# Performance work log

Measured on AMD Instinct MI355X. Metric: run time of the kernel, lower is better.

## Reference

```python
import jax, jax.numpy as jnp
import numpy as np

STRIDES = (8.0, 16.0, 32.0)
ANCHORS = np.array([[[10, 13], [16, 30], [33, 23]],
                    [[30, 61], [62, 45], [59, 119]],
                    [[116, 90], [156, 198], [373, 326]]], dtype=np.float32)
NC = 80
NO = NC + 5
NA = 3
CONF_THRES = 0.15
IOU_THRES = 0.45
MAX_DET = 100
TOPK = 1000          # NMS candidate pre-selection (greedy NMS over top-1000 scores)
MASK_SIZE = 28
MAX_WH = 4096.0      # class offset for batched (class-aware) NMS


def conv(x, w):
    # NCHW conv, stride 1, 'SAME' padding == torch padding=k//2
    return jax.lax.conv_general_dilated(x, w, (1, 1), 'SAME',
                                        dimension_numbers=('NCHW', 'OIHW', 'NCHW'))


def convbn(x, w, g, b, act=False):
    # Conv + (folded) BatchNorm affine + optional SiLU
    y = conv(x, w) * g[None, :, None, None] + b[None, :, None, None]
    return y * jax.nn.sigmoid(y) if act else y


def resize_ac(x, oh, ow):
    # bilinear resize, align_corners=True, NCHW
    H, W = x.shape[-2], x.shape[-1]
    ys = jnp.linspace(0.0, H - 1.0, oh)
    xs = jnp.linspace(0.0, W - 1.0, ow)
    y0 = jnp.floor(ys).astype(jnp.int32); y1 = jnp.minimum(y0 + 1, H - 1)
    x0 = jnp.floor(xs).astype(jnp.int32); x1 = jnp.minimum(x0 + 1, W - 1)
    fy = ys - y0; fx = xs - x0
    rows = x[..., y0, :] * (1.0 - fy)[:, None] + x[..., y1, :] * fy[:, None]
    return rows[..., x0] * (1.0 - fx) + rows[..., x1] * fx


def decode(fraw, anchors_px, stride):
    # fraw: [bs, na*no, ny, nx] -> [bs, na*ny*nx, no] in pixel coords
    bs, _, ny, nx = fraw.shape
    d = fraw.reshape(bs, NA, NO, ny, nx).transpose(0, 1, 3, 4, 2)  # [bs,na,ny,nx,no]
    y = jax.nn.sigmoid(d)
    yv, xv = jnp.meshgrid(jnp.arange(ny, dtype=fraw.dtype),
                          jnp.arange(nx, dtype=fraw.dtype), indexing='ij')
    grid = jnp.stack((xv, yv), -1) - 0.5                 # [ny,nx,2]
    xy = (y[..., :2] * 2.0 + grid) * stride
    wh = (y[..., 2:4] * 2.0) ** 2 * anchors_px[None, :, None, None, :]
    return jnp.concatenate((xy, wh, y[..., 4:]), -1).reshape(bs, -1, NO)


def box_iou(a, b):
    area = lambda t: (t[:, 2] - t[:, 0]) * (t[:, 3] - t[:, 1])
    lt = jnp.maximum(a[:, None, :2], b[None, :, :2])
    rb = jnp.minimum(a[:, None, 2:], b[None, :, 2:])
    wh = jnp.clip(rb - lt, 0.0)
    inter = wh[..., 0] * wh[..., 1]
    return inter / (area(a)[:, None] + area(b)[None, :] - inter + 1e-7)


def nms_image(pred):
    # pred: [N, 85]. conf = obj * cls (multi_label=False -> best class)
    xy = pred[:, :2]; wh = pred[:, 2:4]
    boxes = jnp.concatenate((xy - wh / 2.0, xy + wh / 2.0), -1)
    obj = pred[:, 4]; cls = pred[:, 5:]
    score = obj * jnp.max(cls, -1)
    cls_idx = jnp.argmax(cls, -1)
    s = jnp.where(score > CONF_THRES, score, -1.0)
    sK, idx = jax.lax.top_k(s, TOPK)
    bK = boxes[idx]; cK = cls_idx[idx]
    vK = sK > CONF_THRES
    offb = bK + (cK.astype(bK.dtype) * MAX_WH)[:, None]  # class-aware offset
    iou = box_iou(offb, offb)

    def body(i, st):
        keep, supp = st
        ki = vK[i] & jnp.logical_not(supp[i])
        supp = jnp.where(ki, jnp.logical_or(supp, iou[i] > IOU_THRES), supp)
        return keep.at[i].set(ki), supp

    keep, _ = jax.lax.fori_loop(0, TOPK, body,
                                (jnp.zeros(TOPK, dtype=bool), jnp.zeros(TOPK, dtype=bool)))
    sF = jnp.where(keep, sK, -1.0)
    top_s, top_i = jax.lax.top_k(sF, MAX_DET)
    valid = top_s > 0.0
    out_boxes = bK[top_i] * valid[:, None]
    out_scores = jnp.where(valid, top_s, 0.0)
    out_labels = jnp.where(valid, cK[top_i] + 1, 0)  # 1-based labels
    return out_boxes, out_scores, out_labels, valid


def bilinear_sample(img, ys, xs):
    # img [C,H,W]; ys, xs [P] -> [C,P]; edge-clamped
    H, W = img.shape[-2], img.shape[-1]
    ys = jnp.clip(ys, 0.0, H - 1.0); xs = jnp.clip(xs, 0.0, W - 1.0)
    y0 = jnp.floor(ys).astype(jnp.int32); y1 = jnp.minimum(y0 + 1, H - 1)
    x0 = jnp.floor(xs).astype(jnp.int32); x1 = jnp.minimum(x0 + 1, W - 1)
    ly = ys - y0; lx = xs - x0
    v00 = img[:, y0, x0]; v01 = img[:, y0, x1]
    v10 = img[:, y1, x0]; v11 = img[:, y1, x1]
    return (v00 * (1 - ly) * (1 - lx) + v01 * (1 - ly) * lx +
            v10 * ly * (1 - lx) + v11 * ly * lx)


def roi_align(f, rois, b_idx, out=MASK_SIZE):
    # aligned=False, spatial_scale applied by caller, 1 sample per bin (bin center)
    frac = (jnp.arange(out, dtype=f.dtype) + 0.5) / out

    def one(b, box):
        img = f[b]
        x1, y1, x2, y2 = box[0], box[1], box[2], box[3]
        rw = jnp.maximum(x2 - x1, 1.0); rh = jnp.maximum(y2 - y1, 1.0)
        cx = x1 + frac * rw; cy = y1 + frac * rh
        ys = jnp.repeat(cy, out); xs = jnp.tile(cx, out)
        return bilinear_sample(img, ys, xs).reshape(-1, out, out)

    return jax.vmap(one)(b_idx, rois)


def forward(x0, x1, x2, w_det0, b_det0, w_det1, b_det1, w_det2, b_det2,
            w_seg0, g_seg0, b_seg0, w_seg1, g_seg1, b_seg1, w_seg2, g_seg2, b_seg2,
            w_sc, g_sc, b_sc, w_ml, b_ml):
    feats = (x0, x1, x2)
    wdet = ((w_det0, b_det0), (w_det1, b_det1), (w_det2, b_det2))
    preds = []
    for i in range(3):
        fraw = conv(feats[i], wdet[i][0]) + wdet[i][1][None, :, None, None]
        preds.append(decode(fraw, jnp.asarray(ANCHORS[i]), STRIDES[i]))
    preds = jnp.concatenate(preds, 1)  # [bs, 25200, 85]

    # seg FPN: top-down with align_corners=True bilinear upsample + add
    f = convbn(x2, w_seg0, g_seg0, b_seg0)
    f = resize_ac(f, x1.shape[-2], x1.shape[-1])
    f = convbn(f + x1, w_seg1, g_seg1, b_seg1)
    f = resize_ac(f, x0.shape[-2], x0.shape[-1])
    f = convbn(f + x0, w_seg2, g_seg2, b_seg2)  # [bs, 128, 80, 80]

    boxes, scores, labels, valid = jax.vmap(nms_image)(preds)
    bs = boxes.shape[0]
    rois = jax.lax.stop_gradient(boxes) / STRIDES[0]   # boxes.detach() / stride[0]
    b_idx = jnp.repeat(jnp.arange(bs), MAX_DET)
    crops = roi_align(f, rois.reshape(-1, 4), b_idx)   # [bs*MAX_DET, 128, 28, 28]

    # seg_h: SiLU -> Conv(k=3, act=True) -> 1x1 mask logits
    h = crops * jax.nn.sigmoid(crops)
    h = convbn(h, w_sc, g_sc, b_sc, act=True)
    logits = conv(h, w_ml) + b_ml[None, :, None, None]
    probs = jax.nn.sigmoid(logits)                     # [R, 80, 28, 28]
    lab = jnp.clip(labels.reshape(-1) - 1, 0, NC - 1)  # nc == nc_masks: pick class channel
    masks = probs[jnp.arange(probs.shape[0]), lab]
    masks = masks.reshape(bs, MAX_DET, MASK_SIZE, MASK_SIZE) * valid[..., None, None]
    return boxes, scores, labels, valid, masks


def setup_inputs() -> dict:
    key = jax.random.key(0)
    ks = iter(jax.random.split(key, 48))

    def rn(shape, scale=1.0):
        return jax.random.normal(next(ks), shape, jnp.float32) * scale

    def wconv(o, i, k):
        return rn((o, i, k, k), 1.0 / float(np.sqrt(i * k * k)))

    return {
        'x0': rn((2, 256, 80, 80)),
        'x1': rn((2, 512, 40, 40)),
        'x2': rn((2, 1024, 20, 20)),
        'w_det0': wconv(255, 256, 1), 'b_det0': rn((255,), 0.1),
        'w_det1': wconv(255, 512, 1), 'b_det1': rn((255,), 0.1),
        'w_det2': wconv(255, 1024, 1), 'b_det2': rn((255,), 0.1),
        'w_seg0': wconv(512, 1024, 3), 'g_seg0': jnp.ones(512, jnp.float32), 'b_seg0': rn((512,), 0.1),
        'w_seg1': wconv(256, 512, 3), 'g_seg1': jnp.ones(256, jnp.float32), 'b_seg1': rn((256,), 0.1),
        'w_seg2': wconv(128, 256, 3), 'g_seg2': jnp.ones(128, jnp.float32), 'b_seg2': rn((128,), 0.1),
        'w_sc': wconv(128, 128, 3), 'g_sc': jnp.ones(128, jnp.float32), 'b_sc': rn((128,), 0.1),
        'w_ml': wconv(80, 128, 1), 'b_ml': rn((80,), 0.1),
    }


def reference(x0, x1, x2, w_det0, b_det0, w_det1, b_det1, w_det2, b_det2,
              w_seg0, g_seg0, b_seg0, w_seg1, g_seg1, b_seg1, w_seg2, g_seg2, b_seg2,
              w_sc, g_sc, b_sc, w_ml, b_ml):
    return forward(x0, x1, x2, w_det0, b_det0, w_det1, b_det1, w_det2, b_det2,
                   w_seg0, g_seg0, b_seg0, w_seg1, g_seg1, b_seg1, w_seg2, g_seg2, b_seg2,
                   w_sc, g_sc, b_sc, w_ml, b_ml)
```

## Files before the change

kernel.cpp:

```cpp
#include <hip/hip_runtime.h>
#include <hip/hip_bf16.h>

typedef unsigned int u32;
typedef unsigned long long u64;
typedef short bf16x8 __attribute__((ext_vector_type(8)));
typedef float f32x4 __attribute__((ext_vector_type(4)));

#define NCAND 1000
#define NANCH 25200

__device__ __forceinline__ float sig_acc(float x) { return 1.0f / (1.0f + expf(-x)); }
__device__ __forceinline__ float silu_fast(float v) { return v / (1.0f + __expf(-v)); }
__device__ __forceinline__ unsigned short f2b(float f) {
    __hip_bfloat16 h = __float2bfloat16(f);
    return *reinterpret_cast<unsigned short*>(&h);
}
__device__ __forceinline__ float b2f(unsigned short u) {
    return __uint_as_float(((u32)u) << 16);
}
__device__ __forceinline__ int swz(int p) { return (p & 3) ^ ((p >> 2) & 3); }

__device__ __forceinline__ void gload16(const void* g, void* l) {
    __builtin_amdgcn_global_load_lds((const __attribute__((address_space(1))) void*)g,
                                     (__attribute__((address_space(3))) void*)l, 16, 0, 0);
}

__global__ __launch_bounds__(256) void prep_all_kernel(
    const float* __restrict__ w_det0, const float* __restrict__ w_det1, const float* __restrict__ w_det2,
    float* __restrict__ wdt0, float* __restrict__ wdt1, float* __restrict__ wdt2,
    const float* __restrict__ w_seg0, const float* __restrict__ w_seg1,
    const float* __restrict__ w_seg2, const float* __restrict__ w_sc,
    unsigned short* __restrict__ wp0, unsigned short* __restrict__ wp1,
    unsigned short* __restrict__ wp2, unsigned short* __restrict__ wp3,
    const float* __restrict__ x0, const float* __restrict__ x1, const float* __restrict__ x2,
    unsigned short* __restrict__ x0n, unsigned short* __restrict__ x1n, unsigned short* __restrict__ x2n,
    float* __restrict__ zerobuf)
{
    __shared__ float tile[64][65];
    int b = blockIdx.x, t = threadIdx.x;
    if (b < 112) {
        const float* w; float* wdt; int C, c0, oc0;
        if (b < 16)      { w = w_det0; wdt = wdt0; C = 256;  c0 = (b & 3) * 64;  oc0 = (b >> 2) * 64; }
        else if (b < 48) { int l = b - 16; w = w_det1; wdt = wdt1; C = 512;  c0 = (l & 7) * 64;  oc0 = (l >> 3) * 64; }
        else             { int l = b - 48; w = w_det2; wdt = wdt2; C = 1024; c0 = (l & 15) * 64; oc0 = (l >> 4) * 64; }
        for (int k = t; k < 1024; k += 256) {
            int oo = k >> 4, q = k & 15;
            int oc = oc0 + oo;
            float4 v = {0.f, 0.f, 0.f, 0.f};
            if (oc < 255) v = *(const float4*)&w[(size_t)oc * C + c0 + q * 4];
            tile[oo][q * 4 + 0] = v.x; tile[oo][q * 4 + 1] = v.y;
            tile[oo][q * 4 + 2] = v.z; tile[oo][q * 4 + 3] = v.w;
        }
        __syncthreads();
        for (int k = t; k < 1024; k += 256) {
            int cc = k >> 4, q = k & 15;
            float4 o;
            o.x = tile[q * 4 + 0][cc]; o.y = tile[q * 4 + 1][cc];
            o.z = tile[q * 4 + 2][cc]; o.w = tile[q * 4 + 3][cc];
            *(float4*)&wdt[(size_t)(c0 + cc) * 256 + oc0 + q * 4] = o;
        }
    } else if (b == 112) {
        zerobuf[t] = 0.0f; zerobuf[t + 256] = 0.0f;
    } else if (b < 2865) {
        int l = b - 113;
        const float* w; unsigned short* dst; int Cin, Cout;
        if (l < 2048)      { w = w_seg0; dst = wp0; Cin = 1024; Cout = 512; }
        else if (l < 2560) { l -= 2048; w = w_seg1; dst = wp1; Cin = 512; Cout = 256; }
        else if (l < 2688) { l -= 2560; w = w_seg2; dst = wp2; Cin = 256; Cout = 128; }
        else               { l -= 2688; w = w_sc;  dst = wp3; Cin = 128; Cout = 128; }
        int i = l * 256 + t;
        if (i < Cout * Cin) {
            int oc = i / Cin, c = i - oc * Cin;
            int nch = Cin >> 5;
            int ocb = oc >> 6, ocl = oc & 63, chn = c >> 5, cl = c & 31;
            const float* src = w + (size_t)i * 9;
            size_t base = (((size_t)(ocb * nch + chn) * 9) * 64 + ocl) * 32 + cl;
            #pragma unroll
            for (int tap = 0; tap < 9; tap++)
                dst[base + (size_t)tap * 2048] = f2b(src[tap]);
        }
    } else {
        int l = b - 2865;
        const float* x; unsigned short* y; int C, HW, n, c0, p0;
        if (l < 800)       { x = x0; y = x0n; C = 256;  HW = 6400; p0 = (l % 100) * 64; c0 = ((l / 100) & 3) * 64; n = l / 400; }
        else if (l < 1200) { l -= 800;  x = x1; y = x1n; C = 512;  HW = 1600; p0 = (l % 25) * 64; c0 = ((l / 25) & 7) * 64; n = l / 200; }
        else               { l -= 1200; x = x2; y = x2n; C = 1024; HW = 400;  p0 = (l % 7) * 64;  c0 = ((l / 7) & 15) * 64; n = l / 112; }
        const float* xb = x + ((size_t)n * C + c0) * HW;
        for (int k = t; k < 1024; k += 256) {
            int cc = k >> 4, q = k & 15;
            int gp = p0 + q * 4;
            float4 v = {0.f, 0.f, 0.f, 0.f};
            if (gp < HW) v = *(const float4*)&xb[(size_t)cc * HW + gp];
            tile[cc][q * 4 + 0] = v.x; tile[cc][q * 4 + 1] = v.y;
            tile[cc][q * 4 + 2] = v.z; tile[cc][q * 4 + 3] = v.w;
        }
        __syncthreads();
        for (int k = t; k < 512; k += 256) {
            int pp = k >> 3, cg = k & 7;
            int gp = p0 + pp;
            if (gp < HW) {
                bf16x8 pk;
                #pragma unroll
                for (int j = 0; j < 8; j++) pk[j] = (short)f2b(tile[cg * 8 + j][pp]);
                *(bf16x8*)&y[((size_t)n * HW + gp) * C + c0 + cg * 8] = pk;
            }
        }
    }
}

__global__ __launch_bounds__(256) void det_conv_kernel(
    const float* __restrict__ x, const float* __restrict__ wdt, const float* __restrict__ bias,
    float* __restrict__ dst, int C, int HW, int c_len, int nsl)
{
    int nx = (HW + 127) >> 7;
    int ngroups = nx * nsl * 2;
    int id = blockIdx.x;
    int xcd = id & 7;
    int rest = id >> 3;
    int sub = rest & 7;
    int dgrp = rest >> 3;
    int gidx = dgrp * 8 + xcd;
    if (gidx >= ngroups) return;
    int px = gidx % nx;
    int r0 = gidx / nx;
    int slice = r0 % nsl;
    int b = r0 / nsl;
    int oc0 = sub * 32;
    int px0 = px * 128;
    int c0base = slice * c_len;
    __shared__ float xs[2][32][128];
    __shared__ float wsm[2][32][32];
    int t = threadIdx.x;
    int lane = t & 63, wv = t >> 6;
    int pxg = t & 31, og = t >> 5;
    int lpx = pxg << 2;
    bool full = (px0 + 128 <= HW);
    const float* xb = x + (size_t)b * C * HW;

    auto stage = [&](int c0, int nb) {
        if (full) {
            for (int i = wv; i < 16; i += 4) {
                const float* src = xb + (size_t)(c0 + 2 * i + (lane >> 5)) * HW + px0 + (lane & 31) * 4;
                gload16(src, &xs[nb][2 * i][0]);
            }
        } else {
            for (int k = t; k < 4096; k += 256) {
                int cc = k >> 7, pp = k & 127;
                int gp = px0 + pp;
                xs[nb][cc][pp] = (gp < HW) ? xb[(size_t)(c0 + cc) * HW + gp] : 0.0f;
            }
        }
        const float* wsrc = wdt + (size_t)(c0 + 8 * wv + (lane >> 3)) * 256 + oc0 + (lane & 7) * 4;
        gload16(wsrc, &wsm[nb][8 * wv][0]);
    };

    float acc[4][4] = {{0.f,0.f,0.f,0.f},{0.f,0.f,0.f,0.f},{0.f,0.f,0.f,0.f},{0.f,0.f,0.f,0.f}};
    int nchk = c_len >> 5;
    stage(c0base, 0);
    __syncthreads();
    int nb = 0;
    for (int ch = 0; ch < nchk; ch++) {
        if (ch + 1 < nchk) stage(c0base + ((ch + 1) << 5), nb ^ 1);
        #pragma unroll 8
        for (int cc = 0; cc < 32; cc++) {
            float4 xv = *(const float4*)&xs[nb][cc][lpx];
            float4 wv4 = *(const float4*)&wsm[nb][cc][og << 2];
            float xr[4] = {xv.x, xv.y, xv.z, xv.w};
            float wr[4] = {wv4.x, wv4.y, wv4.z, wv4.w};
            #pragma unroll
            for (int oo = 0; oo < 4; oo++)
                #pragma unroll
                for (int j = 0; j < 4; j++)
                    acc[oo][j] = fmaf(wr[oo], xr[j], acc[oo][j]);
        }
        __syncthreads();
        nb ^= 1;
    }
    float* outb = dst + (size_t)slice * ((size_t)2 * 255 * HW);
    int gp = px0 + lpx;
    #pragma unroll
    for (int oo = 0; oo < 4; oo++) {
        int oc = oc0 + (og << 2) + oo;
        if (oc >= 255) continue;
        float bv = (nsl == 1) ? bias[oc] : 0.0f;
        float* ob = outb + ((size_t)b * 255 + oc) * HW;
        if (gp + 3 < HW) {
            float4 v; v.x = acc[oo][0]+bv; v.y = acc[oo][1]+bv; v.z = acc[oo][2]+bv; v.w = acc[oo][3]+bv;
            *(float4*)&ob[gp] = v;
        } else {
            for (int j = 0; j < 4; j++) if (gp + j < HW) ob[gp + j] = acc[oo][j] + bv;
        }
    }
}

__global__ void det_combine_all_kernel(
    const float* __restrict__ p1, const float* __restrict__ b1, float* __restrict__ co1,
    const float* __restrict__ p2, const float* __restrict__ b2, float* __restrict__ co2)
{
    int b = blockIdx.x, t = threadIdx.x;
    const float* parts; const float* bias; float* co; int nsl, HW, tid, total4;
    if (b < 797) { parts = p1; bias = b1; co = co1; nsl = 2; HW = 1600; tid = b * 256 + t; total4 = 2 * 255 * 1600 / 4; }
    else         { parts = p2; bias = b2; co = co2; nsl = 8; HW = 400;  tid = (b - 797) * 256 + t; total4 = 2 * 255 * 400 / 4; }
    if (tid >= total4) return;
    size_t stride = (size_t)2 * 255 * HW;
    float4 s = {0.f, 0.f, 0.f, 0.f};
    for (int sl = 0; sl < nsl; sl++) {
        float4 v = *(const float4*)&parts[sl * stride + (size_t)tid * 4];
        s.x += v.x; s.y += v.y; s.z += v.z; s.w += v.w;
    }
    int oc = ((tid * 4) / HW) % 255;
    float bv = bias[oc];
    s.x += bv; s.y += bv; s.z += bv; s.w += bv;
    *(float4*)&co[(size_t)tid * 4] = s;
}

__global__ void decode_all_kernel(const float* __restrict__ co0, const float* __restrict__ co1,
    const float* __restrict__ co2, float* __restrict__ boxes_all, u64* __restrict__ keys,
    int* __restrict__ cls_all)
{
    int blk = blockIdx.x, t = threadIdx.x;
    const float* conv; int ny, base, total; float stride;
    float aw0, ah0, aw1, ah1, aw2, ah2;
    int tid;
    if (blk < 150) {
        conv = co0; ny = 80; stride = 8.0f; base = 0; total = 38400;
        aw0 = 10.f; ah0 = 13.f; aw1 = 16.f; ah1 = 30.f; aw2 = 33.f; ah2 = 23.f;
        tid = blk * 256 + t;
    } else if (blk < 188) {
        conv = co1; ny = 40; stride = 16.0f; base = 19200; total = 9600;
        aw0 = 30.f; ah0 = 61.f; aw1 = 62.f; ah1 = 45.f; aw2 = 59.f; ah2 = 119.f;
        tid = (blk - 150) * 256 + t;
    } else {
        conv = co2; ny = 20; stride = 32.0f; base = 24000; total = 2400;
        aw0 = 116.f; ah0 = 90.f; aw1 = 156.f; ah1 = 198.f; aw2 = 373.f; ah2 = 326.f;
        tid = (blk - 188) * 256 + t;
    }
    if (tid >= total) return;
    int nx = ny;
    int HW = ny * nx;
    int gx = tid % nx; int r = tid / nx;
    int gy = r % ny; r /= ny;
    int a = r % 3; int b = r / 3;
    const float* cb = conv + ((size_t)b * 255 + a * 85) * HW + (size_t)gy * nx + gx;
    float v0 = cb[0];
    float v1 = cb[(size_t)1 * HW];
    float v2 = cb[(size_t)2 * HW];
    float v3 = cb[(size_t)3 * HW];
    float v4 = cb[(size_t)4 * HW];
    float mx = cb[(size_t)5 * HW];
    int mi = 0;
    for (int o = 6; o < 85; o++) {
        float q = cb[(size_t)o * HW];
        if (q > mx) { mx = q; mi = o - 5; }
    }
    float aw = (a == 0) ? aw0 : ((a == 1) ? aw1 : aw2);
    float ah = (a == 0) ? ah0 : ((a == 1) ? ah1 : ah2);
    float sx = sig_acc(v0), sy = sig_acc(v1);
    float sw2 = 2.0f * sig_acc(v2), sh2 = 2.0f * sig_acc(v3);
    float cx = (2.0f * sx + ((float)gx - 0.5f)) * stride;
    float cy = (2.0f * sy + ((float)gy - 0.5f)) * stride;
    float bw = sw2 * sw2 * aw;
    float bh = sh2 * sh2 * ah;
    float score = sig_acc(v4) * sig_acc(mx);
    float s = (score > 0.15f) ? score : -1.0f;
    u32 fb = __float_as_uint(s);
    u32 m = (fb & 0x80000000u) ? ~fb : (fb | 0x80000000u);
    int gidx = base + (a * ny + gy) * nx + gx;
    size_t gi = (size_t)b * NANCH + gidx;
    float4 bx;
    bx.x = cx - bw * 0.5f; bx.y = cy - bh * 0.5f;
    bx.z = cx + bw * 0.5f; bx.w = cy + bh * 0.5f;
    *(float4*)&boxes_all[gi * 4] = bx;
    keys[gi] = ((u64)m << 32) | (u64)(0xFFFFFFFFu - (u32)gidx);
    cls_all[gi] = mi;
}

union TKU { u32 h[4][2048]; u64 sortb[2048]; };

__global__ __launch_bounds__(1024) void topk_kernel(
    const u64* __restrict__ keys_all, const float* __restrict__ boxes_all,
    const int* __restrict__ cls_all,
    float* __restrict__ cbox, float* __restrict__ coff,
    float* __restrict__ cscore, int* __restrict__ ccls)
{
    int img = blockIdx.x;
    const u64* keys = keys_all + (size_t)img * NANCH;
    __shared__ TKU sh;
    __shared__ u32 s_prefix;
    __shared__ int s_rank, s_bin, s_cntgt;
    __shared__ u32 s_cnt;
    int t = threadIdx.x;
    if (t == 0) { s_prefix = 0; s_rank = NCAND; }
    __syncthreads();
    u32 maskdone = 0;
    #pragma unroll 1
    for (int pass = 0; pass < 3; pass++) {
        int shift = (pass == 0) ? 21 : ((pass == 1) ? 10 : 0);
        int nbins = (pass == 2) ? 1024 : 2048;
        for (int i = t; i < 4 * 2048; i += 1024) ((u32*)sh.h)[i] = 0;
        __syncthreads();
        u32 pfx = s_prefix;
        for (int i = t; i < NANCH; i += 1024) {
            u32 u = (u32)(keys[i] >> 32);
            if ((u & maskdone) == pfx) atomicAdd(&sh.h[t & 3][(u >> shift) & (nbins - 1)], 1u);
        }
        __syncthreads();
        for (int i = t; i < nbins; i += 1024)
            sh.h[0][i] = sh.h[0][i] + sh.h[1][i] + sh.h[2][i] + sh.h[3][i];
        __syncthreads();
        u32* A = sh.h[0]; u32* B = sh.h[1];
        for (int st = 1; st < nbins; st <<= 1) {
            for (int i = t; i < nbins; i += 1024)
                B[i] = A[i] + ((i + st < nbins) ? A[i + st] : 0u);
            __syncthreads();
            u32* tmp = A; A = B; B = tmp;
        }
        int rk = s_rank;
        for (int i = t; i < nbins; i += 1024) {
            u32 ge = A[i];
            u32 gt = (i + 1 < nbins) ? A[i + 1] : 0u;
            if (ge >= (u32)rk && gt < (u32)rk) { s_bin = i; s_cntgt = (int)gt; }
        }
        __syncthreads();
        if (t == 0) {
            s_prefix |= ((u32)s_bin) << shift;
            s_rank -= s_cntgt;
        }
        maskdone |= (u32)(nbins - 1) << shift;
        __syncthreads();
    }
    u32 pivot = s_prefix;
    if (t == 0) s_cnt = 0;
    __syncthreads();
    for (int i = t; i < NANCH; i += 1024) {
        u64 k = keys[i]; u32 u = (u32)(k >> 32);
        if (u > pivot) { u32 p = atomicAdd(&s_cnt, 1u); sh.sortb[p] = k; }
    }
    __syncthreads();
    for (int i = t; i < NANCH; i += 1024) {
        u64 k = keys[i]; u32 u = (u32)(k >> 32);
        if (u == pivot) { u32 p = atomicAdd(&s_cnt, 1u); if (p < 2048) sh.sortb[p] = k; }
    }
    __syncthreads();
    u32 nc = s_cnt; if (nc > 2048) nc = 2048;
    for (int i = t; i < 2048; i += 1024) if ((u32)i >= nc) sh.sortb[i] = 0ull;
    __syncthreads();
    for (int k = 2; k <= 2048; k <<= 1) {
        for (int j = k >> 1; j > 0; j >>= 1) {
            __syncthreads();
            for (int i = t; i < 2048; i += 1024) {
                int ixj = i ^ j;
                if (ixj > i) {
                    u64 a = sh.sortb[i], c = sh.sortb[ixj];
                    bool first = ((i & k) == 0);
                    if (first ? (a < c) : (a > c)) { sh.sortb[i] = c; sh.sortb[ixj] = a; }
                }
            }
        }
    }
    __syncthreads();
    for (int i = t; i < NCAND; i += 1024) {
        u64 k = sh.sortb[i];
        u32 u = (u32)(k >> 32);
        u32 fb = (u & 0x80000000u) ? (u ^ 0x80000000u) : ~u;
        float s = __uint_as_float(fb);
        int idx = (int)(0xFFFFFFFFu - (u32)k);
        size_t gi = (size_t)img * NANCH + idx;
        float4 bx = *(const float4*)&boxes_all[gi * 4];
        int cl = cls_all[gi];
        int o = img * NCAND + i;
        *(float4*)&cbox[(size_t)o * 4] = bx;
        float off = (float)cl * 4096.0f;
        float4 ob; ob.x = bx.x + off; ob.y = bx.y + off; ob.z = bx.z + off; ob.w = bx.w + off;
        *(float4*)&coff[(size_t)o * 4] = ob;
        cscore[o] = s;
        ccls[o] = cl;
    }
}

__global__ void nms_mask_kernel(const float* __restrict__ coff, u64* __restrict__ maskbuf)
{
    int img = blockIdx.y;
    int tid = blockIdx.x * 256 + threadIdx.x;
    if (tid >= NCAND * 16) return;
    int i = tid >> 4, jw = tid & 15;
    const float* cb = coff + (size_t)img * NCAND * 4;
    float ax1 = cb[i*4+0], ay1 = cb[i*4+1], ax2 = cb[i*4+2], ay2 = cb[i*4+3];
    float aarea = (ax2 - ax1) * (ay2 - ay1);
    u64 bits = 0;
    for (int jj = 0; jj < 64; jj++) {
        int j = jw * 64 + jj;
        if (j >= NCAND) break;
        float bx1 = cb[j*4+0], by1 = cb[j*4+1], bx2 = cb[j*4+2], by2 = cb[j*4+3];
        float barea = (bx2 - bx1) * (by2 - by1);
        float ltx = fmaxf(ax1, bx1), lty = fmaxf(ay1, by1);
        float rbx = fminf(ax2, bx2), rby = fminf(ay2, by2);
        float ww = fmaxf(rbx - ltx, 0.0f), hh = fmaxf(rby - lty, 0.0f);
        float inter = ww * hh;
        float iou = inter / (aarea + barea - inter + 1e-7f);
        if (iou > 0.45f) bits |= (1ull << jj);
    }
    maskbuf[((size_t)img * 1024 + i) * 16 + jw] = bits;
}

__global__ __launch_bounds__(64) void nms_serial_kernel(
    const float* __restrict__ cbox, const float* __restrict__ cscore,
    const int* __restrict__ ccls, const u64* __restrict__ maskbuf,
    float* __restrict__ out, float* __restrict__ rois,
    int* __restrict__ lab, float* __restrict__ validf)
{
    int img = blockIdx.x;
    int lane = threadIdx.x;
    __shared__ float sS[1024];
    for (int i = lane; i < 1024; i += 64)
        sS[i] = (i < NCAND) ? cscore[img * NCAND + i] : -1.0f;
    __syncthreads();
    u64 validw = 0;
    #pragma unroll
    for (int w = 0; w < 16; w++) {
        u64 b = __ballot(sS[w * 64 + lane] > 0.15f);
        if (lane == w) validw = b;
    }
    const u64* mrow = maskbuf + (size_t)img * 1024 * 16;
    int lw = lane & 15;
    u64 rowsel = (lane < 16) ? ~0ull : 0ull;
    u64 suppw = 0, keepw = 0;
    int kcount = 0;
    u64 ring[16];
    #pragma unroll
    for (int k = 0; k < 16; k++) ring[k] = mrow[(size_t)k * 16 + lw];
    for (int ib = 0; ib < 1024; ib += 16) {
        #pragma unroll
        for (int k = 0; k < 16; k++) {
            int i = ib + k;
            u64 row = ring[k];
            ring[k] = mrow[(size_t)((i + 16) & 1023) * 16 + lw];
            int sh = i & 63;
            bool owner_valid = (lane == (i >> 6)) && ((validw >> sh) & 1ull);
            bool mine = owner_valid && !((suppw >> sh) & 1ull);
            u64 bal = __ballot(mine);
            u64 keepall = bal ? ~0ull : 0ull;
            kcount += bal ? 1 : 0;
            suppw |= row & rowsel & keepall;
            keepw |= ((u64)mine) << sh;
        }
        if (kcount >= 100) break;
    }
    int cnt = (lane < 16) ? __popcll(keepw) : 0;
    int pre = 0, total = 0;
    for (int l = 0; l < 16; l++) {
        int c = __shfl(cnt, l);
        if (l < lane) pre += c;
        total += c;
    }
    int kc = total < 100 ? total : 100;
    if (lane < 16) {
        int r = pre;
        u64 kw = keepw;
        while (kw) {
            int b = __ffsll((long long)kw) - 1;
            kw &= kw - 1;
            if (r < 100) {
                int i = lane * 64 + b;
                int ci = img * NCAND + i;
                int slot = img * 100 + r;
                float4 bx = *(const float4*)&cbox[(size_t)ci * 4];
                *(float4*)&out[(size_t)slot * 4] = bx;
                out[800 + slot] = sS[i];
                out[1000 + slot] = (float)(ccls[ci] + 1);
                out[1200 + slot] = 1.0f;
                float4 rv; rv.x = bx.x * 0.125f; rv.y = bx.y * 0.125f; rv.z = bx.z * 0.125f; rv.w = bx.w * 0.125f;
                *(float4*)&rois[(size_t)slot * 4] = rv;
                lab[slot] = ccls[ci];
                validf[slot] = 1.0f;
            }
            r++;
        }
    }
    for (int s = kc + lane; s < 100; s += 64) {
        int slot = img * 100 + s;
        float4 z; z.x = 0; z.y = 0; z.z = 0; z.w = 0;
        *(float4*)&out[(size_t)slot * 4] = z;
        out[800 + slot] = 0.0f;
        out[1000 + slot] = 0.0f;
        out[1200 + slot] = 0.0f;
        *(float4*)&rois[(size_t)slot * 4] = z;
        lab[slot] = 0;
        validf[slot] = 0.0f;
    }
}

#define XBUF 21504
__global__ __launch_bounds__(256) void mfma_conv3x3(
    const unsigned short* __restrict__ in, const unsigned short* __restrict__ wp,
    const float* __restrict__ gain, const float* __restrict__ bias,
    unsigned short* __restrict__ out, const float* __restrict__ zerobuf,
    int Cin, int Cout, int H, int W, int act, int ksl, float* __restrict__ pout)
{
    __shared__ __align__(16) char smem[2 * XBUF];
    int tilesX = (W + 15) >> 4;
    int tilesY = (H + 15) >> 4;
    int tiles = tilesX * tilesY;
    int nocb = Cout >> 6;
    int ngroups = tiles * ksl * 2;
    int id = blockIdx.x;
    int xcd = id & 7;
    int rest = id >> 3;
    int sub = rest % nocb;
    int dgrp = rest / nocb;
    int gidx = dgrp * 8 + xcd;
    if (gidx >= ngroups) return;
    int tile = gidx % tiles;
    int r0 = gidx / tiles;
    int slice = r0 % ksl;
    int n = r0 / ksl;
    int ocb = sub;
    int tY = tile / tilesX, tX = tile - tY * tilesX;
    int y0 = tY << 4, x0 = tX << 4;
    int oc0 = ocb << 6;
    int t = threadIdx.x;
    int lane = t & 63, wv = t >> 6;
    int lg = lane >> 4, lr = lane & 15;
    int HW = H * W;
    int nch = Cin >> 5;
    int nchunks = nch / ksl;
    int chbase = slice * nchunks;
    const unsigned short* inb = in + (size_t)n * HW * Cin;
    const unsigned short* wpb = wp + (size_t)ocb * ((size_t)nch * 9 * 2048);
    int spix = lane >> 2, sg = lane & 3;

    f32x4 acc[4][4];
    #pragma unroll
    for (int p = 0; p < 4; p++)
        #pragma unroll
        for (int q = 0; q < 4; q++)
            acc[p][q] = (f32x4){0.f, 0.f, 0.f, 0.f};

    auto stageX = [&](int ch, int nbuf) {
        int c0 = ch << 5;
        char* dst0 = smem + nbuf * XBUF;
        for (int i = wv; i < 21; i += 4) {
            int pix = i * 16 + spix;
            int yy = (pix * 57) >> 10;
            int xx = pix - yy * 18;
            int gy = y0 - 1 + yy, gx = x0 - 1 + xx;
            bool oob = (pix >= 324) || (gy < 0) || (gy >= H) || (gx < 0) || (gx >= W);
            int gsw = sg ^ swz(pix);
            const void* src = oob ? (const void*)zerobuf
                : (const void*)(inb + (size_t)(gy * W + gx) * Cin + c0 + gsw * 8);
            gload16(src, dst0 + i * 1024);
        }
    };

    stageX(chbase, 0);
    __syncthreads();
    int nb = 0;
    for (int ci = 0; ci < nchunks; ci++) {
        int ch = chbase + ci;
        if (ci + 1 < nchunks) stageX(ch + 1, nb ^ 1);
        const char* sx = smem + nb * XBUF;
        const unsigned short* wsrc = wpb + (size_t)ch * (9 * 2048);
        #pragma unroll 3
        for (int tap = 0; tap < 9; tap++) {
            int dy = tap / 3, dx = tap - dy * 3;
            bf16x8 wf[4];
            #pragma unroll
            for (int q = 0; q < 4; q++)
                wf[q] = *(const bf16x8*)(wsrc + (size_t)(tap * 64 + q * 16 + lr) * 32 + lg * 8);
            #pragma unroll
            for (int p = 0; p < 4; p++) {
                int pix = ((wv << 2) + p + dy) * 18 + dx + lr;
                bf16x8 xf = *(const bf16x8*)(sx + (pix << 6) + ((lg ^ swz(pix)) << 4));
                #pragma unroll
                for (int q = 0; q < 4; q++)
                    acc[p][q] = __builtin_amdgcn_mfma_f32_16x16x32_bf16(wf[q], xf, acc[p][q], 0, 0, 0);
            }
        }
        __syncthreads();
        nb ^= 1;
    }
    int x = x0 + lr;
    if (x >= W) return;
    if (ksl == 1) {
        #pragma unroll
        for (int p = 0; p < 4; p++) {
            int y = y0 + (wv << 2) + p;
            if (y >= H) continue;
            unsigned short* ob = out + ((size_t)n * HW + (size_t)y * W + x) * Cout + oc0;
            #pragma unroll
            for (int q = 0; q < 4; q++) {
                int obase = (q << 4) + (lg << 2);
                ushort4 pk;
                #pragma unroll
                for (int r2 = 0; r2 < 4; r2++) {
                    int oc = oc0 + obase + r2;
                    float v = acc[p][q][r2] * gain[oc] + bias[oc];
                    if (act) v = silu_fast(v);
                    ((unsigned short*)&pk)[r2] = f2b(v);
                }
                *(ushort4*)&ob[obase] = pk;
            }
        }
    } else {
        float* pb = pout + ((size_t)(slice * 2 + n) * HW) * Cout;
        #pragma unroll
        for (int p = 0; p < 4; p++) {
            int y = y0 + (wv << 2) + p;
            if (y >= H) continue;
            float* ob = pb + ((size_t)y * W + x) * Cout + oc0;
            #pragma unroll
            for (int q = 0; q < 4; q++)
                *(f32x4*)&ob[(q << 4) + (lg << 2)] = acc[p][q];
        }
    }
}

#define SC_CHSTRIDE 18432
#define SC_OCBS     73728
__global__ __launch_bounds__(256) void mfma_conv_mask(
    const unsigned short* __restrict__ in, const unsigned short* __restrict__ wp,
    const float* __restrict__ gain, const float* __restrict__ bias,
    const float* __restrict__ wml, const int* __restrict__ lab,
    const float* __restrict__ validf,
    int d0, float* __restrict__ pdot, const float* __restrict__ zerobuf)
{
    __shared__ __align__(16) char smem[XBUF];
    __shared__ float wsh[32];
    int id = blockIdx.x;
    int xcd = id & 7;
    int slot = id >> 3;
    int sub = slot & 15;
    int dgrp = slot >> 4;
    int dl = dgrp * 8 + xcd;
    int d = d0 + dl;
    if (validf[d] == 0.0f) return;
    int tile = sub >> 2, oq = sub & 3;
    int tY = tile >> 1, tX = tile & 1;
    int y0 = tY << 4, x0 = tX << 4;
    int oc0 = oq << 5;
    int ocb64 = oc0 >> 6;
    int olocal = oc0 & 63;
    int t = threadIdx.x;
    int lane = t & 63, wv = t >> 6;
    int lg = lane >> 4, lr = lane & 15;
    const unsigned short* inb = in + (size_t)dl * 784 * 128;
    const unsigned short* wpb = wp + (size_t)ocb64 * SC_OCBS;
    int spix = lane >> 2, sg = lane & 3;
    int L = lab[d];
    if (t < 32) wsh[t] = wml[(size_t)L * 128 + oc0 + t];

    const unsigned short* abase[6];
    #pragma unroll
    for (int s = 0; s < 6; s++) {
        int i = wv + s * 4;
        int pix = i * 16 + spix;
        int yy = (pix * 57) >> 10;
        int xx = pix - yy * 18;
        int gy = y0 - 1 + yy, gx = x0 - 1 + xx;
        bool oob = (i >= 21) || (pix >= 324) || (gy < 0) || (gy >= 28) || (gx < 0) || (gx >= 28);
        int gsw = sg ^ swz(pix);
        abase[s] = oob ? (const unsigned short*)zerobuf
                       : inb + (size_t)(gy * 28 + gx) * 128 + gsw * 8;
    }

    f32x4 acc[4][2];
    #pragma unroll
    for (int p = 0; p < 4; p++)
        #pragma unroll
        for (int q = 0; q < 2; q++)
            acc[p][q] = (f32x4){0.f, 0.f, 0.f, 0.f};

    for (int ch = 0; ch < 4; ch++) {
        {
            int c0 = ch << 5;
            char* dst0 = smem + wv * 1024;
            #pragma unroll
            for (int s = 0; s < 6; s++) {
                int i = wv + s * 4;
                if (i < 21) gload16(abase[s] + c0, dst0 + s * 4096);
            }
        }
        __syncthreads();
        const char* sx = smem;
        const unsigned short* wsrc = wpb + (size_t)ch * SC_CHSTRIDE;
        #pragma unroll 3
        for (int tap = 0; tap < 9; tap++) {
            int dy = tap / 3, dx = tap - dy * 3;
            bf16x8 wf[2];
            #pragma unroll
            for (int q = 0; q < 2; q++)
                wf[q] = *(const bf16x8*)(wsrc + (size_t)(tap * 64 + olocal + q * 16 + lr) * 32 + lg * 8);
            #pragma unroll
            for (int p = 0; p < 4; p++) {
                int pix = ((wv << 2) + p + dy) * 18 + dx + lr;
                bf16x8 xf = *(const bf16x8*)(sx + (pix << 6) + ((lg ^ swz(pix)) << 4));
                #pragma unroll
                for (int q = 0; q < 2; q++)
                    acc[p][q] = __builtin_amdgcn_mfma_f32_16x16x32_bf16(wf[q], xf, acc[p][q], 0, 0, 0);
            }
        }
        __syncthreads();
    }
    int x = x0 + lr;
    #pragma unroll
    for (int p = 0; p < 4; p++) {
        int y = y0 + (wv << 2) + p;
        float part = 0.0f;
        #pragma unroll
        for (int q = 0; q < 2; q++) {
            #pragma unroll
            for (int r2 = 0; r2 < 4; r2++) {
                int ol = (q << 4) + (lg << 2) + r2;
                float v = acc[p][q][r2] * gain[oc0 + ol] + bias[oc0 + ol];
                v = silu_fast(v);
                part = fmaf(wsh[ol], v, part);
            }
        }
        part += __shfl_xor(part, 16);
        part += __shfl_xor(part, 32);
        if (lg == 0 && x < 28 && y < 28)
            pdot[((size_t)oq * 200 + d) * 784 + y * 28 + x] = part;
    }
}

__global__ void mask_combine_kernel(const float* __restrict__ pdot,
    const float* __restrict__ bml, const int* __restrict__ lab,
    const float* __restrict__ validf, float* __restrict__ out)
{
    int tid = blockIdx.x * 256 + threadIdx.x;
    if (tid >= 200 * 784) return;
    int d = tid / 784;
    if (validf[d] == 0.0f) { out[1400 + tid] = 0.0f; return; }
    const size_t S = (size_t)200 * 784;
    float s = pdot[tid] + pdot[S + tid] + pdot[2 * S + tid] + pdot[3 * S + tid] + bml[lab[d]];
    out[1400 + tid] = 1.0f / (1.0f + __expf(-s));
}

__global__ void seg_combine_kernel(const float* __restrict__ parts,
    const float* __restrict__ gain, const float* __restrict__ bias,
    unsigned short* __restrict__ out, int nsl, int total4, int C, int act)
{
    int tid = blockIdx.x * 256 + threadIdx.x;
    if (tid >= total4) return;
    size_t stride = (size_t)total4 * 4;
    float4 s = {0.f, 0.f, 0.f, 0.f};
    for (int sl = 0; sl < nsl; sl++) {
        float4 v = *(const float4*)&parts[sl * stride + (size_t)tid * 4];
        s.x += v.x; s.y += v.y; s.z += v.z; s.w += v.w;
    }
    int oc = (tid * 4) % C;
    float r[4] = {s.x, s.y, s.z, s.w};
    ushort4 pk;
    #pragma unroll
    for (int j = 0; j < 4; j++) {
        float v = r[j] * gain[oc + j] + bias[oc + j];
        if (act) v = silu_fast(v);
        ((unsigned short*)&pk)[j] = f2b(v);
    }
    *(ushort4*)&out[(size_t)tid * 4] = pk;
}

__global__ void resize_add_kernel(const unsigned short* __restrict__ f,
    const unsigned short* __restrict__ skip, unsigned short* __restrict__ out,
    int C8, int C, int IH, int IW, int OH, int OW)
{
    int tid = blockIdx.x * 256 + threadIdx.x;
    int total = 2 * OH * OW * C8;
    if (tid >= total) return;
    int cg = tid % C8; int r = tid / C8;
    int ox = r % OW; r /= OW;
    int oy = r % OH; int n = r / OH;
    float sy = (float)(IH - 1) / (float)(OH - 1);
    float sx = (float)(IW - 1) / (float)(OW - 1);
    float ys = oy * sy, xs = ox * sx;
    int y0 = (int)floorf(ys); if (y0 > IH - 1) y0 = IH - 1;
    int x0 = (int)floorf(xs); if (x0 > IW - 1) x0 = IW - 1;
    int y1 = min(y0 + 1, IH - 1), x1 = min(x0 + 1, IW - 1);
    float fy = ys - (float)y0, fx = xs - (float)x0;
    const unsigned short* fb = f + (size_t)n * IH * IW * C + cg * 8;
    bf16x8 a00 = *(const bf16x8*)&fb[(size_t)(y0 * IW + x0) * C];
    bf16x8 a01 = *(const bf16x8*)&fb[(size_t)(y0 * IW + x1) * C];
    bf16x8 a10 = *(const bf16x8*)&fb[(size_t)(y1 * IW + x0) * C];
    bf16x8 a11 = *(const bf16x8*)&fb[(size_t)(y1 * IW + x1) * C];
    bf16x8 sk = *(const bf16x8*)&skip[(size_t)tid * 8];
    bf16x8 o;
    #pragma unroll
    for (int j = 0; j < 8; j++) {
        float r0 = b2f((unsigned short)a00[j]) * (1.0f - fy) + b2f((unsigned short)a10[j]) * fy;
        float r1 = b2f((unsigned short)a01[j]) * (1.0f - fy) + b2f((unsigned short)a11[j]) * fy;
        float v = r0 * (1.0f - fx) + r1 * fx + b2f((unsigned short)sk[j]);
        o[j] = (short)f2b(v);
    }
    *(bf16x8*)&out[(size_t)tid * 8] = o;
}

__global__ void roi_silu_kernel(const unsigned short* __restrict__ fseg,
    const float* __restrict__ rois, const float* __restrict__ validf,
    int d0, int total, unsigned short* __restrict__ hbuf)
{
    int tid = blockIdx.x * 256 + threadIdx.x;
    if (tid >= total) return;
    int cg = tid & 15; int r = tid >> 4;
    int p = r % 784; int dl = r / 784;
    int d = d0 + dl; int b = d / 100;
    if (validf[d] == 0.0f) return;
    int py = p / 28, px = p % 28;
    const float* ro = rois + (size_t)d * 4;
    float x1 = ro[0], y1 = ro[1], x2 = ro[2], y2 = ro[3];
    float rw = fmaxf(x2 - x1, 1.0f), rh = fmaxf(y2 - y1, 1.0f);
    float cx = x1 + (((float)px + 0.5f) / 28.0f) * rw;
    float cy = y1 + (((float)py + 0.5f) / 28.0f) * rh;
    cx = fminf(fmaxf(cx, 0.0f), 79.0f);
    cy = fminf(fmaxf(cy, 0.0f), 79.0f);
    int ix0 = (int)floorf(cx), iy0 = (int)floorf(cy);
    int ix1 = min(ix0 + 1, 79), iy1 = min(iy0 + 1, 79);
    float lx = cx - (float)ix0, ly = cy - (float)iy0;
    const unsigned short* fb = fseg + (size_t)b * 6400 * 128 + cg * 8;
    bf16x8 v00 = *(const bf16x8*)&fb[(size_t)(iy0 * 80 + ix0) * 128];
    bf16x8 v01 = *(const bf16x8*)&fb[(size_t)(iy0 * 80 + ix1) * 128];
    bf16x8 v10 = *(const bf16x8*)&fb[(size_t)(iy1 * 80 + ix0) * 128];
    bf16x8 v11 = *(const bf16x8*)&fb[(size_t)(iy1 * 80 + ix1) * 128];
    float w00 = (1.0f - ly) * (1.0f - lx), w01 = (1.0f - ly) * lx;
    float w10 = ly * (1.0f - lx), w11 = ly * lx;
    bf16x8 o;
    #pragma unroll
    for (int j = 0; j < 8; j++) {
        float v = b2f((unsigned short)v00[j]) * w00 + b2f((unsigned short)v01[j]) * w01
                + b2f((unsigned short)v10[j]) * w10 + b2f((unsigned short)v11[j]) * w11;
        o[j] = (short)f2b(silu_fast(v));
    }
    *(bf16x8*)&hbuf[((size_t)dl * 784 + p) * 128 + cg * 8] = o;
}


extern "C" void kernel_launch(void* const* d_in, const int* in_sizes, int n_in,
                              void* d_out, int out_size, void* d_ws, size_t ws_size,
                              hipStream_t stream)
{
    const float* x0 = (const float*)d_in[0];
    const float* x1 = (const float*)d_in[1];
    const float* x2 = (const float*)d_in[2];
    const float* w_det0 = (const float*)d_in[3];
    const float* b_det0 = (const float*)d_in[4];
    const float* w_det1 = (const float*)d_in[5];
    const float* b_det1 = (const float*)d_in[6];
    const float* w_det2 = (const float*)d_in[7];
    const float* b_det2 = (const float*)d_in[8];
    const float* w_seg0 = (const float*)d_in[9];
    const float* g_seg0 = (const float*)d_in[10];
    const float* b_seg0 = (const float*)d_in[11];
    const float* w_seg1 = (const float*)d_in[12];
    const float* g_seg1 = (const float*)d_in[13];
    const float* b_seg1 = (const float*)d_in[14];
    const float* w_seg2 = (const float*)d_in[15];
    const float* g_seg2 = (const float*)d_in[16];
    const float* b_seg2 = (const float*)d_in[17];
    const float* w_sc = (const float*)d_in[18];
    const float* g_sc = (const float*)d_in[19];
    const float* b_sc = (const float*)d_in[20];
    const float* w_ml = (const float*)d_in[21];
    const float* b_ml = (const float*)d_in[22];
    float* out = (float*)d_out;

    char* ws = (char*)d_ws;
    size_t off = 0;
    auto alloc = [&](size_t bytes) -> void* {
        off = (off + 255) & ~(size_t)255;
        void* p = ws + off;
        off += bytes;
        return p;
    };
    float* co0    = (float*)alloc((size_t)2 * 255 * 6400 * 4);
    float* co1    = (float*)alloc((size_t)2 * 255 * 1600 * 4);
    float* co2    = (float*)alloc((size_t)2 * 255 * 400 * 4);
    float* boxesA = (float*)alloc((size_t)2 * NANCH * 4 * 4);
    u64*   keysA  = (u64*)  alloc((size_t)2 * NANCH * 8);
    int*   clsA   = (int*)  alloc((size_t)2 * NANCH * 4);
    float* cbox   = (float*)alloc((size_t)2 * NCAND * 4 * 4);
    float* coffb  = (float*)alloc((size_t)2 * NCAND * 4 * 4);
    float* cscore = (float*)alloc((size_t)2 * NCAND * 4);
    int*   ccls   = (int*)  alloc((size_t)2 * NCAND * 4);
    u64*   maskb  = (u64*)  alloc((size_t)2 * 1024 * 16 * 8);
    float* wdt0   = (float*)alloc((size_t)256 * 256 * 4);
    float* wdt1   = (float*)alloc((size_t)512 * 256 * 4);
    float* wdt2   = (float*)alloc((size_t)1024 * 256 * 4);
    unsigned short* x0n = (unsigned short*)alloc((size_t)2 * 6400 * 256 * 2);
    unsigned short* x1n = (unsigned short*)alloc((size_t)2 * 1600 * 512 * 2);
    unsigned short* x2n = (unsigned short*)alloc((size_t)2 * 400 * 1024 * 2);
    const size_t s0 = (size_t)512 * 1024 * 9, s1 = (size_t)256 * 512 * 9,
                 s2 = (size_t)128 * 256 * 9,  s3 = (size_t)128 * 128 * 9;
    unsigned short* wprep = (unsigned short*)alloc((s0 + s1 + s2 + s3) * 2);
    float* pbuf = (float*)alloc((size_t)4 * 2 * 1600 * 256 * 4);
    float* pbuf2 = pbuf + (size_t)2 * 2 * 255 * 1600;
    unsigned short* f0   = (unsigned short*)alloc((size_t)2 * 400 * 512 * 2);
    unsigned short* r1b  = (unsigned short*)alloc((size_t)2 * 1600 * 512 * 2);
    unsigned short* f1   = (unsigned short*)alloc((size_t)2 * 1600 * 256 * 2);
    unsigned short* r2b  = (unsigned short*)alloc((size_t)2 * 6400 * 256 * 2);
    unsigned short* fseg = (unsigned short*)alloc((size_t)2 * 6400 * 128 * 2);
    float* zerobuf = (float*)alloc(2048);
    float* roisW  = (float*)alloc((size_t)200 * 4 * 4);
    int*   labW   = (int*)  alloc((size_t)200 * 4);
    float* validW = (float*)alloc((size_t)200 * 4);
    float* pdot   = (float*)alloc((size_t)4 * 200 * 784 * 4);
    unsigned short* hbuf   = (unsigned short*)alloc((size_t)200 * 784 * 128 * 2);

    int DCH = 200;
    if (off > ws_size) {
        DCH = 25;
        hbuf = (unsigned short*)co0;
    }

    prep_all_kernel<<<4289, 256, 0, stream>>>(
        w_det0, w_det1, w_det2, wdt0, wdt1, wdt2,
        w_seg0, w_seg1, w_seg2, w_sc,
        wprep, wprep + s0, wprep + s0 + s1, wprep + s0 + s1 + s2,
        x0, x1, x2, x0n, x1n, x2n, zerobuf);

    det_conv_kernel<<<832, 256, 0, stream>>>(x0, wdt0, b_det0, co0, 256, 6400, 256, 1);
    det_conv_kernel<<<448, 256, 0, stream>>>(x1, wdt1, b_det1, pbuf, 512, 1600, 256, 2);
    det_conv_kernel<<<512, 256, 0, stream>>>(x2, wdt2, b_det2, pbuf2, 1024, 400, 128, 8);
    det_combine_all_kernel<<<997, 256, 0, stream>>>(pbuf, b_det1, co1, pbuf2, b_det2, co2);

    decode_all_kernel<<<198, 256, 0, stream>>>(co0, co1, co2, boxesA, keysA, clsA);

    topk_kernel<<<2, 1024, 0, stream>>>(keysA, boxesA, clsA, cbox, coffb, cscore, ccls);
    nms_mask_kernel<<<dim3((NCAND * 16 + 255) / 256, 2), 256, 0, stream>>>(coffb, maskb);
    nms_serial_kernel<<<2, 64, 0, stream>>>(cbox, cscore, ccls, maskb, out, roisW, labW, validW);

    mfma_conv3x3<<<256, 256, 0, stream>>>(x2n, wprep, g_seg0, b_seg0, f0, zerobuf, 1024, 512, 20, 20, 0, 4, pbuf);
    seg_combine_kernel<<<(2*400*512/4 + 255)/256, 256, 0, stream>>>(pbuf, g_seg0, b_seg0, f0, 4, 2*400*512/4, 512, 0);
    resize_add_kernel<<<(2 * 1600 * 64 + 255) / 256, 256, 0, stream>>>(f0, x1n, r1b, 64, 512, 20, 20, 40, 40);
    mfma_conv3x3<<<288, 256, 0, stream>>>(r1b, wprep + s0, g_seg1, b_seg1, f1, zerobuf, 512, 256, 40, 40, 0, 4, pbuf);
    seg_combine_kernel<<<(2*1600*256/4 + 255)/256, 256, 0, stream>>>(pbuf, g_seg1, b_seg1, f1, 4, 2*1600*256/4, 256, 0);
    resize_add_kernel<<<(2 * 6400 * 32 + 255) / 256, 256, 0, stream>>>(f1, x0n, r2b, 32, 256, 40, 40, 80, 80);
    mfma_conv3x3<<<208, 256, 0, stream>>>(r2b, wprep + s0 + s1, g_seg2, b_seg2, fseg, zerobuf, 256, 128, 80, 80, 0, 2, pbuf);
    seg_combine_kernel<<<(2*6400*128/4 + 255)/256, 256, 0, stream>>>(pbuf, g_seg2, b_seg2, fseg, 2, 2*6400*128/4, 128, 0);

    for (int d0i = 0; d0i < 200; d0i += DCH) {
        int total = DCH * 784 * 16;
        roi_silu_kernel<<<(total + 255) / 256, 256, 0, stream>>>(fseg, roisW, validW, d0i, total, hbuf);
        mfma_conv_mask<<<DCH * 16, 256, 0, stream>>>(hbuf, wprep + s0 + s1 + s2,
            g_sc, b_sc, w_ml, labW, validW, d0i, pdot, zerobuf);
    }
    mask_combine_kernel<<<(200 * 784 + 255) / 256, 256, 0, stream>>>(pdot, b_ml, labW, validW, out);
}
```

Baseline: 452.6 us.

## Merge detection convs and co-schedule NMS stages with segmentation branch kernels

Merges the three detection 1x1 conv launches into one grid and folds the split-K partial sum plus bias into the decode kernel, which removes the separate combine pass. It also packs the independent top-k, NMS mask and serial NMS work into the same launches as the first seg conv, its combine and the resize, using block-index dispatch. The aim is fewer launches and letting the small serial detection stages overlap with the segmentation work. In exchange, decode now reads up to 8 partial buffers per channel, and the fused kernels run 1024-thread blocks in which some threads sit idle during the conv phase.

```diff
diff --git a/kernel.cpp b/kernel.cpp
--- a/kernel.cpp
+++ b/kernel.cpp
@@ -108,13 +108,20 @@
     }
 }
 
-__global__ __launch_bounds__(256) void det_conv_kernel(
-    const float* __restrict__ x, const float* __restrict__ wdt, const float* __restrict__ bias,
-    float* __restrict__ dst, int C, int HW, int c_len, int nsl)
-{
+__global__ __launch_bounds__(256) void det_conv_all_kernel(
+    const float* __restrict__ xa, const float* __restrict__ wdta, const float* __restrict__ ba, float* __restrict__ da,
+    const float* __restrict__ xb2, const float* __restrict__ wdtb, const float* __restrict__ bb, float* __restrict__ db,
+    const float* __restrict__ xc, const float* __restrict__ wdtc, const float* __restrict__ bc, float* __restrict__ dc)
+{
+    const float* x; const float* wdt; const float* bias; float* dst;
+    int C, HW, c_len, nsl, id;
+    int blk = blockIdx.x;
+    if (blk < 832)       { x = xa;  wdt = wdta; bias = ba; dst = da; C = 256;  HW = 6400; c_len = 256; nsl = 1; id = blk; }
+    else if (blk < 1280) { x = xb2; wdt = wdtb; bias = bb; dst = db; C = 512;  HW = 1600; c_len = 256; nsl = 2; id = blk - 832; }
+    else                 { x = xc;  wdt = wdtc; bias = bc; dst = dc; C = 1024; HW = 400;  c_len = 128; nsl = 8; id = blk - 1280; }
+
     int nx = (HW + 127) >> 7;
     int ngroups = nx * nsl * 2;
-    int id = blockIdx.x;
     int xcd = id & 7;
     int rest = id >> 3;
     int sub = rest & 7;
@@ -193,45 +200,28 @@
     }
 }
 
-__global__ void det_combine_all_kernel(
-    const float* __restrict__ p1, const float* __restrict__ b1, float* __restrict__ co1,
-    const float* __restrict__ p2, const float* __restrict__ b2, float* __restrict__ co2)
-{
-    int b = blockIdx.x, t = threadIdx.x;
-    const float* parts; const float* bias; float* co; int nsl, HW, tid, total4;
-    if (b < 797) { parts = p1; bias = b1; co = co1; nsl = 2; HW = 1600; tid = b * 256 + t; total4 = 2 * 255 * 1600 / 4; }
-    else         { parts = p2; bias = b2; co = co2; nsl = 8; HW = 400;  tid = (b - 797) * 256 + t; total4 = 2 * 255 * 400 / 4; }
-    if (tid >= total4) return;
-    size_t stride = (size_t)2 * 255 * HW;
-    float4 s = {0.f, 0.f, 0.f, 0.f};
-    for (int sl = 0; sl < nsl; sl++) {
-        float4 v = *(const float4*)&parts[sl * stride + (size_t)tid * 4];
-        s.x += v.x; s.y += v.y; s.z += v.z; s.w += v.w;
-    }
-    int oc = ((tid * 4) / HW) % 255;
-    float bv = bias[oc];
-    s.x += bv; s.y += bv; s.z += bv; s.w += bv;
-    *(float4*)&co[(size_t)tid * 4] = s;
-}
-
-__global__ void decode_all_kernel(const float* __restrict__ co0, const float* __restrict__ co1,
-    const float* __restrict__ co2, float* __restrict__ boxes_all, u64* __restrict__ keys,
-    int* __restrict__ cls_all)
+__global__ void decode_all_kernel(const float* __restrict__ co0,
+    const float* __restrict__ p1, const float* __restrict__ bd1,
+    const float* __restrict__ p2, const float* __restrict__ bd2,
+    float* __restrict__ boxes_all, u64* __restrict__ keys, int* __restrict__ cls_all)
 {
     int blk = blockIdx.x, t = threadIdx.x;
-    const float* conv; int ny, base, total; float stride;
+    const float* parts = co0; const float* bias = bd1;
+    int ny, base, total, nsl; float stride; size_t sstride = 0;
     float aw0, ah0, aw1, ah1, aw2, ah2;
     int tid;
     if (blk < 150) {
-        conv = co0; ny = 80; stride = 8.0f; base = 0; total = 38400;
+        nsl = 1; ny = 80; stride = 8.0f; base = 0; total = 38400;
         aw0 = 10.f; ah0 = 13.f; aw1 = 16.f; ah1 = 30.f; aw2 = 33.f; ah2 = 23.f;
         tid = blk * 256 + t;
     } else if (blk < 188) {
-        conv = co1; ny = 40; stride = 16.0f; base = 19200; total = 9600;
+        parts = p1; bias = bd1; nsl = 2; sstride = (size_t)2 * 255 * 1600;
+        ny = 40; stride = 16.0f; base = 19200; total = 9600;
         aw0 = 30.f; ah0 = 61.f; aw1 = 62.f; ah1 = 45.f; aw2 = 59.f; ah2 = 119.f;
         tid = (blk - 150) * 256 + t;
     } else {
-        conv = co2; ny = 20; stride = 32.0f; base = 24000; total = 2400;
+        parts = p2; bias = bd2; nsl = 8; sstride = (size_t)2 * 255 * 400;
+        ny = 20; stride = 32.0f; base = 24000; total = 2400;
         aw0 = 116.f; ah0 = 90.f; aw1 = 156.f; ah1 = 198.f; aw2 = 373.f; ah2 = 326.f;
         tid = (blk - 188) * 256 + t;
     }
@@ -241,16 +231,25 @@
     int gx = tid % nx; int r = tid / nx;
     int gy = r % ny; r /= ny;
     int a = r % 3; int b = r / 3;
-    const float* cb = conv + ((size_t)b * 255 + a * 85) * HW + (size_t)gy * nx + gx;
-    float v0 = cb[0];
-    float v1 = cb[(size_t)1 * HW];
-    float v2 = cb[(size_t)2 * HW];
-    float v3 = cb[(size_t)3 * HW];
-    float v4 = cb[(size_t)4 * HW];
-    float mx = cb[(size_t)5 * HW];
+    size_t idx0 = ((size_t)b * 255 + a * 85) * HW + (size_t)gy * nx + gx;
+
+    auto rd = [&](int o) -> float {
+        size_t ix = idx0 + (size_t)o * HW;
+        if (nsl == 1) return co0[ix];
+        float s = 0.f;
+        for (int sl = 0; sl < nsl; sl++) s += parts[(size_t)sl * sstride + ix];
+        return s + bias[a * 85 + o];
+    };
+
+    float v0 = rd(0);
+    float v1 = rd(1);
+    float v2 = rd(2);
+    float v3 = rd(3);
+    float v4 = rd(4);
+    float mx = rd(5);
     int mi = 0;
     for (int o = 6; o < 85; o++) {
-        float q = cb[(size_t)o * HW];
+        float q = rd(o);
         if (q > mx) { mx = q; mi = o - 5; }
     }
     float aw = (a == 0) ? aw0 : ((a == 1) ? aw1 : aw2);
@@ -275,235 +274,19 @@
     cls_all[gi] = mi;
 }
 
-union TKU { u32 h[4][2048]; u64 sortb[2048]; };
-
-__global__ __launch_bounds__(1024) void topk_kernel(
-    const u64* __restrict__ keys_all, const float* __restrict__ boxes_all,
-    const int* __restrict__ cls_all,
-    float* __restrict__ cbox, float* __restrict__ coff,
-    float* __restrict__ cscore, int* __restrict__ ccls)
-{
-    int img = blockIdx.x;
-    const u64* keys = keys_all + (size_t)img * NANCH;
-    __shared__ TKU sh;
-    __shared__ u32 s_prefix;
-    __shared__ int s_rank, s_bin, s_cntgt;
-    __shared__ u32 s_cnt;
-    int t = threadIdx.x;
-    if (t == 0) { s_prefix = 0; s_rank = NCAND; }
-    __syncthreads();
-    u32 maskdone = 0;
-    #pragma unroll 1
-    for (int pass = 0; pass < 3; pass++) {
-        int shift = (pass == 0) ? 21 : ((pass == 1) ? 10 : 0);
-        int nbins = (pass == 2) ? 1024 : 2048;
-        for (int i = t; i < 4 * 2048; i += 1024) ((u32*)sh.h)[i] = 0;
-        __syncthreads();
-        u32 pfx = s_prefix;
-        for (int i = t; i < NANCH; i += 1024) {
-            u32 u = (u32)(keys[i] >> 32);
-            if ((u & maskdone) == pfx) atomicAdd(&sh.h[t & 3][(u >> shift) & (nbins - 1)], 1u);
-        }
-        __syncthreads();
-        for (int i = t; i < nbins; i += 1024)
-            sh.h[0][i] = sh.h[0][i] + sh.h[1][i] + sh.h[2][i] + sh.h[3][i];
-        __syncthreads();
-        u32* A = sh.h[0]; u32* B = sh.h[1];
-        for (int st = 1; st < nbins; st <<= 1) {
-            for (int i = t; i < nbins; i += 1024)
-                B[i] = A[i] + ((i + st < nbins) ? A[i + st] : 0u);
-            __syncthreads();
-            u32* tmp = A; A = B; B = tmp;
-        }
-        int rk = s_rank;
-        for (int i = t; i < nbins; i += 1024) {
-            u32 ge = A[i];
-            u32 gt = (i + 1 < nbins) ? A[i + 1] : 0u;
-            if (ge >= (u32)rk && gt < (u32)rk) { s_bin = i; s_cntgt = (int)gt; }
-        }
-        __syncthreads();
-        if (t == 0) {
-            s_prefix |= ((u32)s_bin) << shift;
-            s_rank -= s_cntgt;
-        }
-        maskdone |= (u32)(nbins - 1) << shift;
-        __syncthreads();
-    }
-    u32 pivot = s_prefix;
-    if (t == 0) s_cnt = 0;
-    __syncthreads();
-    for (int i = t; i < NANCH; i += 1024) {
-        u64 k = keys[i]; u32 u = (u32)(k >> 32);
-        if (u > pivot) { u32 p = atomicAdd(&s_cnt, 1u); sh.sortb[p] = k; }
-    }
-    __syncthreads();
-    for (int i = t; i < NANCH; i += 1024) {
-        u64 k = keys[i]; u32 u = (u32)(k >> 32);
-        if (u == pivot) { u32 p = atomicAdd(&s_cnt, 1u); if (p < 2048) sh.sortb[p] = k; }
-    }
-    __syncthreads();
-    u32 nc = s_cnt; if (nc > 2048) nc = 2048;
-    for (int i = t; i < 2048; i += 1024) if ((u32)i >= nc) sh.sortb[i] = 0ull;
-    __syncthreads();
-    for (int k = 2; k <= 2048; k <<= 1) {
-        for (int j = k >> 1; j > 0; j >>= 1) {
-            __syncthreads();
-            for (int i = t; i < 2048; i += 1024) {
-                int ixj = i ^ j;
-                if (ixj > i) {
-                    u64 a = sh.sortb[i], c = sh.sortb[ixj];
-                    bool first = ((i & k) == 0);
-                    if (first ? (a < c) : (a > c)) { sh.sortb[i] = c; sh.sortb[ixj] = a; }
-                }
-            }
-        }
-    }
-    __syncthreads();
-    for (int i = t; i < NCAND; i += 1024) {
-        u64 k = sh.sortb[i];
-        u32 u = (u32)(k >> 32);
-        u32 fb = (u & 0x80000000u) ? (u ^ 0x80000000u) : ~u;
-        float s = __uint_as_float(fb);
-        int idx = (int)(0xFFFFFFFFu - (u32)k);
-        size_t gi = (size_t)img * NANCH + idx;
-        float4 bx = *(const float4*)&boxes_all[gi * 4];
-        int cl = cls_all[gi];
-        int o = img * NCAND + i;
-        *(float4*)&cbox[(size_t)o * 4] = bx;
-        float off = (float)cl * 4096.0f;
-        float4 ob; ob.x = bx.x + off; ob.y = bx.y + off; ob.z = bx.z + off; ob.w = bx.w + off;
-        *(float4*)&coff[(size_t)o * 4] = ob;
-        cscore[o] = s;
-        ccls[o] = cl;
-    }
-}
-
-__global__ void nms_mask_kernel(const float* __restrict__ coff, u64* __restrict__ maskbuf)
-{
-    int img = blockIdx.y;
-    int tid = blockIdx.x * 256 + threadIdx.x;
-    if (tid >= NCAND * 16) return;
-    int i = tid >> 4, jw = tid & 15;
-    const float* cb = coff + (size_t)img * NCAND * 4;
-    float ax1 = cb[i*4+0], ay1 = cb[i*4+1], ax2 = cb[i*4+2], ay2 = cb[i*4+3];
-    float aarea = (ax2 - ax1) * (ay2 - ay1);
-    u64 bits = 0;
-    for (int jj = 0; jj < 64; jj++) {
-        int j = jw * 64 + jj;
-        if (j >= NCAND) break;
-        float bx1 = cb[j*4+0], by1 = cb[j*4+1], bx2 = cb[j*4+2], by2 = cb[j*4+3];
-        float barea = (bx2 - bx1) * (by2 - by1);
-        float ltx = fmaxf(ax1, bx1), lty = fmaxf(ay1, by1);
-        float rbx = fminf(ax2, bx2), rby = fminf(ay2, by2);
-        float ww = fmaxf(rbx - ltx, 0.0f), hh = fmaxf(rby - lty, 0.0f);
-        float inter = ww * hh;
-        float iou = inter / (aarea + barea - inter + 1e-7f);
-        if (iou > 0.45f) bits |= (1ull << jj);
-    }
-    maskbuf[((size_t)img * 1024 + i) * 16 + jw] = bits;
-}
-
-__global__ __launch_bounds__(64) void nms_serial_kernel(
-    const float* __restrict__ cbox, const float* __restrict__ cscore,
-    const int* __restrict__ ccls, const u64* __restrict__ maskbuf,
-    float* __restrict__ out, float* __restrict__ rois,
-    int* __restrict__ lab, float* __restrict__ validf)
-{
-    int img = blockIdx.x;
-    int lane = threadIdx.x;
-    __shared__ float sS[1024];
-    for (int i = lane; i < 1024; i += 64)
-        sS[i] = (i < NCAND) ? cscore[img * NCAND + i] : -1.0f;
-    __syncthreads();
-    u64 validw = 0;
-    #pragma unroll
-    for (int w = 0; w < 16; w++) {
-        u64 b = __ballot(sS[w * 64 + lane] > 0.15f);
-        if (lane == w) validw = b;
-    }
-    const u64* mrow = maskbuf + (size_t)img * 1024 * 16;
-    int lw = lane & 15;
-    u64 rowsel = (lane < 16) ? ~0ull : 0ull;
-    u64 suppw = 0, keepw = 0;
-    int kcount = 0;
-    u64 ring[16];
-    #pragma unroll
-    for (int k = 0; k < 16; k++) ring[k] = mrow[(size_t)k * 16 + lw];
-    for (int ib = 0; ib < 1024; ib += 16) {
-        #pragma unroll
-        for (int k = 0; k < 16; k++) {
-            int i = ib + k;
-            u64 row = ring[k];
-            ring[k] = mrow[(size_t)((i + 16) & 1023) * 16 + lw];
-            int sh = i & 63;
-            bool owner_valid = (lane == (i >> 6)) && ((validw >> sh) & 1ull);
-            bool mine = owner_valid && !((suppw >> sh) & 1ull);
-            u64 bal = __ballot(mine);
-            u64 keepall = bal ? ~0ull : 0ull;
-            kcount += bal ? 1 : 0;
-            suppw |= row & rowsel & keepall;
-            keepw |= ((u64)mine) << sh;
-        }
-        if (kcount >= 100) break;
-    }
-    int cnt = (lane < 16) ? __popcll(keepw) : 0;
-    int pre = 0, total = 0;
-    for (int l = 0; l < 16; l++) {
-        int c = __shfl(cnt, l);
-        if (l < lane) pre += c;
-        total += c;
-    }
-    int kc = total < 100 ? total : 100;
-    if (lane < 16) {
-        int r = pre;
-        u64 kw = keepw;
-        while (kw) {
-            int b = __ffsll((long long)kw) - 1;
-            kw &= kw - 1;
-            if (r < 100) {
-                int i = lane * 64 + b;
-                int ci = img * NCAND + i;
-                int slot = img * 100 + r;
-                float4 bx = *(const float4*)&cbox[(size_t)ci * 4];
-                *(float4*)&out[(size_t)slot * 4] = bx;
-                out[800 + slot] = sS[i];
-                out[1000 + slot] = (float)(ccls[ci] + 1);
-                out[1200 + slot] = 1.0f;
-                float4 rv; rv.x = bx.x * 0.125f; rv.y = bx.y * 0.125f; rv.z = bx.z * 0.125f; rv.w = bx.w * 0.125f;
-                *(float4*)&rois[(size_t)slot * 4] = rv;
-                lab[slot] = ccls[ci];
-                validf[slot] = 1.0f;
-            }
-            r++;
-        }
-    }
-    for (int s = kc + lane; s < 100; s += 64) {
-        int slot = img * 100 + s;
-        float4 z; z.x = 0; z.y = 0; z.z = 0; z.w = 0;
-        *(float4*)&out[(size_t)slot * 4] = z;
-        out[800 + slot] = 0.0f;
-        out[1000 + slot] = 0.0f;
-        out[1200 + slot] = 0.0f;
-        *(float4*)&rois[(size_t)slot * 4] = z;
-        lab[slot] = 0;
-        validf[slot] = 0.0f;
-    }
-}
-
 #define XBUF 21504
-__global__ __launch_bounds__(256) void mfma_conv3x3(
+__device__ __forceinline__ void conv3x3_body(int id, char* smem,
     const unsigned short* __restrict__ in, const unsigned short* __restrict__ wp,
     const float* __restrict__ gain, const float* __restrict__ bias,
     unsigned short* __restrict__ out, const float* __restrict__ zerobuf,
     int Cin, int Cout, int H, int W, int act, int ksl, float* __restrict__ pout)
 {
-    __shared__ __align__(16) char smem[2 * XBUF];
+    bool on = (threadIdx.x < 256);
     int tilesX = (W + 15) >> 4;
     int tilesY = (H + 15) >> 4;
     int tiles = tilesX * tilesY;
     int nocb = Cout >> 6;
     int ngroups = tiles * ksl * 2;
-    int id = blockIdx.x;
     int xcd = id & 7;
     int rest = id >> 3;
     int sub = rest % nocb;
@@ -552,33 +335,36 @@
         }
     };
 
-    stageX(chbase, 0);
+    if (on) stageX(chbase, 0);
     __syncthreads();
     int nb = 0;
     for (int ci = 0; ci < nchunks; ci++) {
         int ch = chbase + ci;
-        if (ci + 1 < nchunks) stageX(ch + 1, nb ^ 1);
-        const char* sx = smem + nb * XBUF;
-        const unsigned short* wsrc = wpb + (size_t)ch * (9 * 2048);
-        #pragma unroll 3
-        for (int tap = 0; tap < 9; tap++) {
-            int dy = tap / 3, dx = tap - dy * 3;
-            bf16x8 wf[4];
-            #pragma unroll
-            for (int q = 0; q < 4; q++)
-                wf[q] = *(const bf16x8*)(wsrc + (size_t)(tap * 64 + q * 16 + lr) * 32 + lg * 8);
-            #pragma unroll
-            for (int p = 0; p < 4; p++) {
-                int pix = ((wv << 2) + p + dy) * 18 + dx + lr;
-                bf16x8 xf = *(const bf16x8*)(sx + (pix << 6) + ((lg ^ swz(pix)) << 4));
+        if (on && ci + 1 < nchunks) stageX(ch + 1, nb ^ 1);
+        if (on) {
+            const char* sx = smem + nb * XBUF;
+            const unsigned short* wsrc = wpb + (size_t)ch * (9 * 2048);
+            #pragma unroll 3
+            for (int tap = 0; tap < 9; tap++) {
+                int dy = tap / 3, dx = tap - dy * 3;
+                bf16x8 wf[4];
                 #pragma unroll
                 for (int q = 0; q < 4; q++)
-                    acc[p][q] = __builtin_amdgcn_mfma_f32_16x16x32_bf16(wf[q], xf, acc[p][q], 0, 0, 0);
+                    wf[q] = *(const bf16x8*)(wsrc + (size_t)(tap * 64 + q * 16 + lr) * 32 + lg * 8);
+                #pragma unroll
+                for (int p = 0; p < 4; p++) {
+                    int pix = ((wv << 2) + p + dy) * 18 + dx + lr;
+                    bf16x8 xf = *(const bf16x8*)(sx + (pix << 6) + ((lg ^ swz(pix)) << 4));
+                    #pragma unroll
+                    for (int q = 0; q < 4; q++)
+                        acc[p][q] = __builtin_amdgcn_mfma_f32_16x16x32_bf16(wf[q], xf, acc[p][q], 0, 0, 0);
+                }
             }
         }
         __syncthreads();
         nb ^= 1;
     }
+    if (!on) return;
     int x = x0 + lr;
     if (x >= W) return;
     if (ksl == 1) {
@@ -615,132 +401,133 @@
     }
 }
 
-#define SC_CHSTRIDE 18432
-#define SC_OCBS     73728
-__global__ __launch_bounds__(256) void mfma_conv_mask(
+__global__ __launch_bounds__(256) void mfma_conv3x3(
     const unsigned short* __restrict__ in, const unsigned short* __restrict__ wp,
     const float* __restrict__ gain, const float* __restrict__ bias,
-    const float* __restrict__ wml, const int* __restrict__ lab,
-    const float* __restrict__ validf,
-    int d0, float* __restrict__ pdot, const float* __restrict__ zerobuf)
-{
-    __shared__ __align__(16) char smem[XBUF];
-    __shared__ float wsh[32];
-    int id = blockIdx.x;
-    int xcd = id & 7;
-    int slot = id >> 3;
-    int sub = slot & 15;
-    int dgrp = slot >> 4;
-    int dl = dgrp * 8 + xcd;
-    int d = d0 + dl;
-    if (validf[d] == 0.0f) return;
-    int tile = sub >> 2, oq = sub & 3;
-    int tY = tile >> 1, tX = tile & 1;
-    int y0 = tY << 4, x0 = tX << 4;
-    int oc0 = oq << 5;
-    int ocb64 = oc0 >> 6;
-    int olocal = oc0 & 63;
+    unsigned short* __restrict__ out, const float* __restrict__ zerobuf,
+    int Cin, int Cout, int H, int W, int act, int ksl, float* __restrict__ pout)
+{
+    __shared__ __align__(16) char smem[2 * XBUF];
+    conv3x3_body(blockIdx.x, smem, in, wp, gain, bias, out, zerobuf, Cin, Cout, H, W, act, ksl, pout);
+}
+
+union TKU { u32 h[4][2048]; u64 sortb[2048]; };
+
+__global__ __launch_bounds__(1024) void topk_seg0_kernel(
+    const u64* __restrict__ keys_all, const float* __restrict__ boxes_all,
+    const int* __restrict__ cls_all,
+    float* __restrict__ cbox, float* __restrict__ coff,
+    float* __restrict__ cscore, int* __restrict__ ccls,
+    const unsigned short* __restrict__ x2n, const unsigned short* __restrict__ wp0,
+    const float* __restrict__ g_seg0, const float* __restrict__ b_seg0,
+    unsigned short* __restrict__ f0, const float* __restrict__ zerobuf,
+    float* __restrict__ pbuf)
+{
+    __shared__ __align__(16) char ms[2 * XBUF];
+    __shared__ u32 s_prefix;
+    __shared__ int s_rank, s_bin, s_cntgt;
+    __shared__ u32 s_cnt;
+    if (blockIdx.x >= 2) {
+        conv3x3_body((int)blockIdx.x - 2, ms, x2n, wp0, g_seg0, b_seg0, f0, zerobuf,
+                     1024, 512, 20, 20, 0, 4, pbuf);
+        return;
+    }
+    TKU& sh = *(TKU*)ms;
+    int img = blockIdx.x;
+    const u64* keys = keys_all + (size_t)img * NANCH;
     int t = threadIdx.x;
-    int lane = t & 63, wv = t >> 6;
-    int lg = lane >> 4, lr = lane & 15;
-    const unsigned short* inb = in + (size_t)dl * 784 * 128;
-    const unsigned short* wpb = wp + (size_t)ocb64 * SC_OCBS;
-    int spix = lane >> 2, sg = lane & 3;
-    int L = lab[d];
-    if (t < 32) wsh[t] = wml[(size_t)L * 128 + oc0 + t];
-
-    const unsigned short* abase[6];
-    #pragma unroll
-    for (int s = 0; s < 6; s++) {
-        int i = wv + s * 4;
-        int pix = i * 16 + spix;
-        int yy = (pix * 57) >> 10;
-        int xx = pix - yy * 18;
-        int gy = y0 - 1 + yy, gx = x0 - 1 + xx;
-        bool oob = (i >= 21) || (pix >= 324) || (gy < 0) || (gy >= 28) || (gx < 0) || (gx >= 28);
-        int gsw = sg ^ swz(pix);
-        abase[s] = oob ? (const unsigned short*)zerobuf
-                       : inb + (size_t)(gy * 28 + gx) * 128 + gsw * 8;
-    }
-
-    f32x4 acc[4][2];
-    #pragma unroll
-    for (int p = 0; p < 4; p++)
-        #pragma unroll
-        for (int q = 0; q < 2; q++)
-            acc[p][q] = (f32x4){0.f, 0.f, 0.f, 0.f};
-
-    for (int ch = 0; ch < 4; ch++) {
-        {
-            int c0 = ch << 5;
-            char* dst0 = smem + wv * 1024;
-            #pragma unroll
-            for (int s = 0; s < 6; s++) {
-                int i = wv + s * 4;
-                if (i < 21) gload16(abase[s] + c0, dst0 + s * 4096);
+    if (t == 0) { s_prefix = 0; s_rank = NCAND; }
+    __syncthreads();
+    u32 maskdone = 0;
+    #pragma unroll 1
+    for (int pass = 0; pass < 3; pass++) {
+        int shift = (pass == 0) ? 21 : ((pass == 1) ? 10 : 0);
+        int nbins = (pass == 2) ? 1024 : 2048;
+        for (int i = t; i < 4 * 2048; i += 1024) ((u32*)sh.h)[i] = 0;
+        __syncthreads();
+        u32 pfx = s_prefix;
+        for (int i = t; i < NANCH; i += 1024) {
+            u32 u = (u32)(keys[i] >> 32);
+            if ((u & maskdone) == pfx) atomicAdd(&sh.h[t & 3][(u >> shift) & (nbins - 1)], 1u);
+        }
+        __syncthreads();
+        for (int i = t; i < nbins; i += 1024)
+            sh.h[0][i] = sh.h[0][i] + sh.h[1][i] + sh.h[2][i] + sh.h[3][i];
+        __syncthreads();
+        u32* A = sh.h[0]; u32* B = sh.h[1];
+        for (int st = 1; st < nbins; st <<= 1) {
+            for (int i = t; i < nbins; i += 1024)
+                B[i] = A[i] + ((i + st < nbins) ? A[i + st] : 0u);
+            __syncthreads();
+            u32* tmp = A; A = B; B = tmp;
+        }
+        int rk = s_rank;
+        for (int i = t; i < nbins; i += 1024) {
+            u32 ge = A[i];
+            u32 gt = (i + 1 < nbins) ? A[i + 1] : 0u;
+            if (ge >= (u32)rk && gt < (u32)rk) { s_bin = i; s_cntgt = (int)gt; }
+        }
+        __syncthreads();
+        if (t == 0) {
+            s_prefix |= ((u32)s_bin) << shift;
+            s_rank -= s_cntgt;
+        }
+        maskdone |= (u32)(nbins - 1) << shift;
+        __syncthreads();
+    }
+    u32 pivot = s_prefix;
+    if (t == 0) s_cnt = 0;
+    __syncthreads();
+    for (int i = t; i < NANCH; i += 1024) {
+        u64 k = keys[i]; u32 u = (u32)(k >> 32);
+        if (u > pivot) { u32 p = atomicAdd(&s_cnt, 1u); sh.sortb[p] = k; }
+    }
+    __syncthreads();
+    for (int i = t; i < NANCH; i += 1024) {
+        u64 k = keys[i]; u32 u = (u32)(k >> 32);
+        if (u == pivot) { u32 p = atomicAdd(&s_cnt, 1u); if (p < 2048) sh.sortb[p] = k; }
+    }
+    __syncthreads();
+    u32 nc = s_cnt; if (nc > 2048) nc = 2048;
+    for (int i = t; i < 2048; i += 1024) if ((u32)i >= nc) sh.sortb[i] = 0ull;
+    __syncthreads();
+    for (int k = 2; k <= 2048; k <<= 1) {
+        for (int j = k >> 1; j > 0; j >>= 1) {
+            __syncthreads();
+            for (int i = t; i < 2048; i += 1024) {
+                int ixj = i ^ j;
+                if (ixj > i) {
+                    u64 a = sh.sortb[i], c = sh.sortb[ixj];
+                    bool first = ((i & k) == 0);
+                    if (first ? (a < c) : (a > c)) { sh.sortb[i] = c; sh.sortb[ixj] = a; }
+                }
             }
         }
-        __syncthreads();
-        const char* sx = smem;
-        const unsigned short* wsrc = wpb + (size_t)ch * SC_CHSTRIDE;
-        #pragma unroll 3
-        for (int tap = 0; tap < 9; tap++) {
-            int dy = tap / 3, dx = tap - dy * 3;
-            bf16x8 wf[2];
-            #pragma unroll
-            for (int q = 0; q < 2; q++)
-                wf[q] = *(const bf16x8*)(wsrc + (size_t)(tap * 64 + olocal + q * 16 + lr) * 32 + lg * 8);
-            #pragma unroll
-            for (int p = 0; p < 4; p++) {
-                int pix = ((wv << 2) + p + dy) * 18 + dx + lr;
-                bf16x8 xf = *(const bf16x8*)(sx + (pix << 6) + ((lg ^ swz(pix)) << 4));
-                #pragma unroll
-                for (int q = 0; q < 2; q++)
-                    acc[p][q] = __builtin_amdgcn_mfma_f32_16x16x32_bf16(wf[q], xf, acc[p][q], 0, 0, 0);
-            }
-        }
-        __syncthreads();
-    }
-    int x = x0 + lr;
-    #pragma unroll
-    for (int p = 0; p < 4; p++) {
-        int y = y0 + (wv << 2) + p;
-        float part = 0.0f;
-        #pragma unroll
-        for (int q = 0; q < 2; q++) {
-            #pragma unroll
-            for (int r2 = 0; r2 < 4; r2++) {
-                int ol = (q << 4) + (lg << 2) + r2;
-                float v = acc[p][q][r2] * gain[oc0 + ol] + bias[oc0 + ol];
-                v = silu_fast(v);
-                part = fmaf(wsh[ol], v, part);
-            }
-        }
-        part += __shfl_xor(part, 16);
-        part += __shfl_xor(part, 32);
-        if (lg == 0 && x < 28 && y < 28)
-            pdot[((size_t)oq * 200 + d) * 784 + y * 28 + x] = part;
-    }
-}
-
-__global__ void mask_combine_kernel(const float* __restrict__ pdot,
-    const float* __restrict__ bml, const int* __restrict__ lab,
-    const float* __restrict__ validf, float* __restrict__ out)
-{
-    int tid = blockIdx.x * 256 + threadIdx.x;
-    if (tid >= 200 * 784) return;
-    int d = tid / 784;
-    if (validf[d] == 0.0f) { out[1400 + tid] = 0.0f; return; }
-    const size_t S = (size_t)200 * 784;
-    float s = pdot[tid] + pdot[S + tid] + pdot[2 * S + tid] + pdot[3 * S + tid] + bml[lab[d]];
-    out[1400 + tid] = 1.0f / (1.0f + __expf(-s));
-}
-
-__global__ void seg_combine_kernel(const float* __restrict__ parts,
+    }
+    __syncthreads();
+    for (int i = t; i < NCAND; i += 1024) {
+        u64 k = sh.sortb[i];
+        u32 u = (u32)(k >> 32);
+        u32 fb = (u & 0x80000000u) ? (u ^ 0x80000000u) : ~u;
+        float s = __uint_as_float(fb);
+        int idx = (int)(0xFFFFFFFFu - (u32)k);
+        size_t gi = (size_t)img * NANCH + idx;
+        float4 bx = *(const float4*)&boxes_all[gi * 4];
+        int cl = cls_all[gi];
+        int o = img * NCAND + i;
+        *(float4*)&cbox[(size_t)o * 4] = bx;
+        float off = (float)cl * 4096.0f;
+        float4 ob; ob.x = bx.x + off; ob.y = bx.y + off; ob.z = bx.z + off; ob.w = bx.w + off;
+        *(float4*)&coff[(size_t)o * 4] = ob;
+        cscore[o] = s;
+        ccls[o] = cl;
+    }
+}
+
+__device__ __forceinline__ void seg_combine_body(int tid, const float* __restrict__ parts,
     const float* __restrict__ gain, const float* __restrict__ bias,
     unsigned short* __restrict__ out, int nsl, int total4, int C, int act)
 {
-    int tid = blockIdx.x * 256 + threadIdx.x;
     if (tid >= total4) return;
     size_t stride = (size_t)total4 * 4;
     float4 s = {0.f, 0.f, 0.f, 0.f};
@@ -760,11 +547,50 @@
     *(ushort4*)&out[(size_t)tid * 4] = pk;
 }
 
-__global__ void resize_add_kernel(const unsigned short* __restrict__ f,
+__global__ void seg_combine_kernel(const float* __restrict__ parts,
+    const float* __restrict__ gain, const float* __restrict__ bias,
+    unsigned short* __restrict__ out, int nsl, int total4, int C, int act)
+{
+    seg_combine_body(blockIdx.x * 256 + threadIdx.x, parts, gain, bias, out, nsl, total4, C, act);
+}
+
+__global__ __launch_bounds__(256) void nmsmask_comb0_kernel(
+    const float* __restrict__ coff, u64* __restrict__ maskbuf,
+    const float* __restrict__ parts, const float* __restrict__ gain,
+    const float* __restrict__ bias, unsigned short* __restrict__ outb)
+{
+    int blk = blockIdx.x, t = threadIdx.x;
+    if (blk >= 126) {
+        seg_combine_body((blk - 126) * 256 + t, parts, gain, bias, outb, 4, 2*400*512/4, 512, 0);
+        return;
+    }
+    int img = blk / 63;
+    int tid = (blk % 63) * 256 + t;
+    if (tid >= NCAND * 16) return;
+    int i = tid >> 4, jw = tid & 15;
+    const float* cb = coff + (size_t)img * NCAND * 4;
+    float ax1 = cb[i*4+0], ay1 = cb[i*4+1], ax2 = cb[i*4+2], ay2 = cb[i*4+3];
+    float aarea = (ax2 - ax1) * (ay2 - ay1);
+    u64 bits = 0;
+    for (int jj = 0; jj < 64; jj++) {
+        int j = jw * 64 + jj;
+        if (j >= NCAND) break;
+        float bx1 = cb[j*4+0], by1 = cb[j*4+1], bx2 = cb[j*4+2], by2 = cb[j*4+3];
+        float barea = (bx2 - bx1) * (by2 - by1);
+        float ltx = fmaxf(ax1, bx1), lty = fmaxf(ay1, by1);
+        float rbx = fminf(ax2, bx2), rby = fminf(ay2, by2);
+        float ww = fmaxf(rbx - ltx, 0.0f), hh = fmaxf(rby - lty, 0.0f);
+        float inter = ww * hh;
+        float iou = inter / (aarea + barea - inter + 1e-7f);
+        if (iou > 0.45f) bits |= (1ull << jj);
+    }
+    maskbuf[((size_t)img * 1024 + i) * 16 + jw] = bits;
+}
+
+__device__ __forceinline__ void resize_add_body(int tid, const unsigned short* __restrict__ f,
     const unsigned short* __restrict__ skip, unsigned short* __restrict__ out,
     int C8, int C, int IH, int IW, int OH, int OW)
 {
-    int tid = blockIdx.x * 256 + threadIdx.x;
     int total = 2 * OH * OW * C8;
     if (tid >= total) return;
     int cg = tid % C8; int r = tid / C8;
@@ -792,6 +618,229 @@
         o[j] = (short)f2b(v);
     }
     *(bf16x8*)&out[(size_t)tid * 8] = o;
+}
+
+__global__ void resize_add_kernel(const unsigned short* __restrict__ f,
+    const unsigned short* __restrict__ skip, unsigned short* __restrict__ out,
+    int C8, int C, int IH, int IW, int OH, int OW)
+{
+    resize_add_body(blockIdx.x * 256 + threadIdx.x, f, skip, out, C8, C, IH, IW, OH, OW);
+}
+
+__global__ __launch_bounds__(256) void nmsserial_resize1_kernel(
+    const float* __restrict__ cbox, const float* __restrict__ cscore,
+    const int* __restrict__ ccls, const u64* __restrict__ maskbuf,
+    float* __restrict__ out, float* __restrict__ rois,
+    int* __restrict__ lab, float* __restrict__ validf,
+    const unsigned short* __restrict__ f0, const unsigned short* __restrict__ x1n,
+    unsigned short* __restrict__ r1b)
+{
+    __shared__ float sS[1024];
+    int t = threadIdx.x;
+    if (blockIdx.x >= 2) {
+        resize_add_body(((int)blockIdx.x - 2) * 256 + t, f0, x1n, r1b, 64, 512, 20, 20, 40, 40);
+        return;
+    }
+    int img = blockIdx.x;
+    for (int i = t; i < 1024; i += 256)
+        sS[i] = (i < NCAND) ? cscore[img * NCAND + i] : -1.0f;
+    __syncthreads();
+    if (t >= 64) return;
+    int lane = t;
+    u64 validw = 0;
+    #pragma unroll
+    for (int w = 0; w < 16; w++) {
+        u64 b = __ballot(sS[w * 64 + lane] > 0.15f);
+        if (lane == w) validw = b;
+    }
+    const u64* mrow = maskbuf + (size_t)img * 1024 * 16;
+    int lw = lane & 15;
+    u64 rowsel = (lane < 16) ? ~0ull : 0ull;
+    u64 suppw = 0, keepw = 0;
+    int kcount = 0;
+    u64 ring[16];
+    #pragma unroll
+    for (int k = 0; k < 16; k++) ring[k] = mrow[(size_t)k * 16 + lw];
+    for (int ib = 0; ib < 1024; ib += 16) {
+        #pragma unroll
+        for (int k = 0; k < 16; k++) {
+            int i = ib + k;
+            u64 row = ring[k];
+            ring[k] = mrow[(size_t)((i + 16) & 1023) * 16 + lw];
+            int sh = i & 63;
+            bool owner_valid = (lane == (i >> 6)) && ((validw >> sh) & 1ull);
+            bool mine = owner_valid && !((suppw >> sh) & 1ull);
+            u64 bal = __ballot(mine);
+            u64 keepall = bal ? ~0ull : 0ull;
+            kcount += bal ? 1 : 0;
+            suppw |= row & rowsel & keepall;
+            keepw |= ((u64)mine) << sh;
+        }
+        if (kcount >= 100) break;
+    }
+    int cnt = (lane < 16) ? __popcll(keepw) : 0;
+    int pre = 0, total = 0;
+    for (int l = 0; l < 16; l++) {
+        int c = __shfl(cnt, l);
+        if (l < lane) pre += c;
+        total += c;
+    }
+    int kc = total < 100 ? total : 100;
+    if (lane < 16) {
+        int r = pre;
+        u64 kw = keepw;
+        while (kw) {
+            int b = __ffsll((long long)kw) - 1;
+            kw &= kw - 1;
+            if (r < 100) {
+                int i = lane * 64 + b;
+                int ci = img * NCAND + i;
+                int slot = img * 100 + r;
+                float4 bx = *(const float4*)&cbox[(size_t)ci * 4];
+                *(float4*)&out[(size_t)slot * 4] = bx;
+                out[800 + slot] = sS[i];
+                out[1000 + slot] = (float)(ccls[ci] + 1);
+                out[1200 + slot] = 1.0f;
+                float4 rv; rv.x = bx.x * 0.125f; rv.y = bx.y * 0.125f; rv.z = bx.z * 0.125f; rv.w = bx.w * 0.125f;
+                *(float4*)&rois[(size_t)slot * 4] = rv;
+                lab[slot] = ccls[ci];
+                validf[slot] = 1.0f;
+            }
+            r++;
+        }
+    }
+    for (int s = kc + lane; s < 100; s += 64) {
+        int slot = img * 100 + s;
+        float4 z; z.x = 0; z.y = 0; z.z = 0; z.w = 0;
+        *(float4*)&out[(size_t)slot * 4] = z;
+        out[800 + slot] = 0.0f;
+        out[1000 + slot] = 0.0f;
+        out[1200 + slot] = 0.0f;
+        *(float4*)&rois[(size_t)slot * 4] = z;
+        lab[slot] = 0;
+        validf[slot] = 0.0f;
+    }
+}
+
+#define SC_CHSTRIDE 18432
+#define SC_OCBS     73728
+__global__ __launch_bounds__(256) void mfma_conv_mask(
+    const unsigned short* __restrict__ in, const unsigned short* __restrict__ wp,
+    const float* __restrict__ gain, const float* __restrict__ bias,
+    const float* __restrict__ wml, const int* __restrict__ lab,
+    const float* __restrict__ validf,
+    int d0, float* __restrict__ pdot, const float* __restrict__ zerobuf)
+{
+    __shared__ __align__(16) char smem[XBUF];
+    __shared__ float wsh[32];
+    int id = blockIdx.x;
+    int xcd = id & 7;
+    int slot = id >> 3;
+    int sub = slot & 15;
+    int dgrp = slot >> 4;
+    int dl = dgrp * 8 + xcd;
+    int d = d0 + dl;
+    if (validf[d] == 0.0f) return;
+    int tile = sub >> 2, oq = sub & 3;
+    int tY = tile >> 1, tX = tile & 1;
+    int y0 = tY << 4, x0 = tX << 4;
+    int oc0 = oq << 5;
+    int ocb64 = oc0 >> 6;
+    int olocal = oc0 & 63;
+    int t = threadIdx.x;
+    int lane = t & 63, wv = t >> 6;
+    int lg = lane >> 4, lr = lane & 15;
+    const unsigned short* inb = in + (size_t)dl * 784 * 128;
+    const unsigned short* wpb = wp + (size_t)ocb64 * SC_OCBS;
+    int spix = lane >> 2, sg = lane & 3;
+    int L = lab[d];
+    if (t < 32) wsh[t] = wml[(size_t)L * 128 + oc0 + t];
+
+    const unsigned short* abase[6];
+    #pragma unroll
+    for (int s = 0; s < 6; s++) {
+        int i = wv + s * 4;
+        int pix = i * 16 + spix;
+        int yy = (pix * 57) >> 10;
+        int xx = pix - yy * 18;
+        int gy = y0 - 1 + yy, gx = x0 - 1 + xx;
+        bool oob = (i >= 21) || (pix >= 324) || (gy < 0) || (gy >= 28) || (gx < 0) || (gx >= 28);
+        int gsw = sg ^ swz(pix);
+        abase[s] = oob ? (const unsigned short*)zerobuf
+                       : inb + (size_t)(gy * 28 + gx) * 128 + gsw * 8;
+    }
+
+    f32x4 acc[4][2];
+    #pragma unroll
+    for (int p = 0; p < 4; p++)
+        #pragma unroll
+        for (int q = 0; q < 2; q++)
+            acc[p][q] = (f32x4){0.f, 0.f, 0.f, 0.f};
+
+    for (int ch = 0; ch < 4; ch++) {
+        {
+            int c0 = ch << 5;
+            char* dst0 = smem + wv * 1024;
+            #pragma unroll
+            for (int s = 0; s < 6; s++) {
+                int i = wv + s * 4;
+                if (i < 21) gload16(abase[s] + c0, dst0 + s * 4096);
+            }
+        }
+        __syncthreads();
+        const char* sx = smem;
+        const unsigned short* wsrc = wpb + (size_t)ch * SC_CHSTRIDE;
+        #pragma unroll 3
+        for (int tap = 0; tap < 9; tap++) {
+            int dy = tap / 3, dx = tap - dy * 3;
+            bf16x8 wf[2];
+            #pragma unroll
+            for (int q = 0; q < 2; q++)
+                wf[q] = *(const bf16x8*)(wsrc + (size_t)(tap * 64 + olocal + q * 16 + lr) * 32 + lg * 8);
+            #pragma unroll
+            for (int p = 0; p < 4; p++) {
+                int pix = ((wv << 2) + p + dy) * 18 + dx + lr;
+                bf16x8 xf = *(const bf16x8*)(sx + (pix << 6) + ((lg ^ swz(pix)) << 4));
+                #pragma unroll
+                for (int q = 0; q < 2; q++)
+                    acc[p][q] = __builtin_amdgcn_mfma_f32_16x16x32_bf16(wf[q], xf, acc[p][q], 0, 0, 0);
+            }
+        }
+        __syncthreads();
+    }
+    int x = x0 + lr;
+    #pragma unroll
+    for (int p = 0; p < 4; p++) {
+        int y = y0 + (wv << 2) + p;
+        float part = 0.0f;
+        #pragma unroll
+        for (int q = 0; q < 2; q++) {
+            #pragma unroll
+            for (int r2 = 0; r2 < 4; r2++) {
+                int ol = (q << 4) + (lg << 2) + r2;
+                float v = acc[p][q][r2] * gain[oc0 + ol] + bias[oc0 + ol];
+                v = silu_fast(v);
+                part = fmaf(wsh[ol], v, part);
+            }
+        }
+        part += __shfl_xor(part, 16);
+        part += __shfl_xor(part, 32);
+        if (lg == 0 && x < 28 && y < 28)
+            pdot[((size_t)oq * 200 + d) * 784 + y * 28 + x] = part;
+    }
+}
+
+__global__ void mask_combine_kernel(const float* __restrict__ pdot,
+    const float* __restrict__ bml, const int* __restrict__ lab,
+    const float* __restrict__ validf, float* __restrict__ out)
+{
+    int tid = blockIdx.x * 256 + threadIdx.x;
+    if (tid >= 200 * 784) return;
+    int d = tid / 784;
+    if (validf[d] == 0.0f) { out[1400 + tid] = 0.0f; return; }
+    const size_t S = (size_t)200 * 784;
+    float s = pdot[tid] + pdot[S + tid] + pdot[2 * S + tid] + pdot[3 * S + tid] + bml[lab[d]];
+    out[1400 + tid] = 1.0f / (1.0f + __expf(-s));
 }
 
 __global__ void roi_silu_kernel(const unsigned short* __restrict__ fseg,
@@ -916,25 +965,29 @@
         wprep, wprep + s0, wprep + s0 + s1, wprep + s0 + s1 + s2,
         x0, x1, x2, x0n, x1n, x2n, zerobuf);
 
-    det_conv_kernel<<<832, 256, 0, stream>>>(x0, wdt0, b_det0, co0, 256, 6400, 256, 1);
-    det_conv_kernel<<<448, 256, 0, stream>>>(x1, wdt1, b_det1, pbuf, 512, 1600, 256, 2);
-    det_conv_kernel<<<512, 256, 0, stream>>>(x2, wdt2, b_det2, pbuf2, 1024, 400, 128, 8);
-    det_combine_all_kernel<<<997, 256, 0, stream>>>(pbuf, b_det1, co1, pbuf2, b_det2, co2);
-
-    decode_all_kernel<<<198, 256, 0, stream>>>(co0, co1, co2, boxesA, keysA, clsA);
-
-    topk_kernel<<<2, 1024, 0, stream>>>(keysA, boxesA, clsA, cbox, coffb, cscore, ccls);
-    nms_mask_kernel<<<dim3((NCAND * 16 + 255) / 256, 2), 256, 0, stream>>>(coffb, maskb);
-    nms_serial_kernel<<<2, 64, 0, stream>>>(cbox, cscore, ccls, maskb, out, roisW, labW, validW);
-
-    mfma_conv3x3<<<256, 256, 0, stream>>>(x2n, wprep, g_seg0, b_seg0, f0, zerobuf, 1024, 512, 20, 20, 0, 4, pbuf);
-    seg_combine_kernel<<<(2*400*512/4 + 255)/256, 256, 0, stream>>>(pbuf, g_seg0, b_seg0, f0, 4, 2*400*512/4, 512, 0);
-    resize_add_kernel<<<(2 * 1600 * 64 + 255) / 256, 256, 0, stream>>>(f0, x1n, r1b, 64, 512, 20, 20, 40, 40);
+    det_conv_all_kernel<<<1792, 256, 0, stream>>>(
+        x0, wdt0, b_det0, co0,
+        x1, wdt1, b_det1, pbuf,
+        x2, wdt2, b_det2, pbuf2);
+
+    decode_all_kernel<<<198, 256, 0, stream>>>(co0, pbuf, b_det1, pbuf2, b_det2,
+                                               boxesA, keysA, clsA);
+
+    topk_seg0_kernel<<<258, 1024, 0, stream>>>(keysA, boxesA, clsA,
+        cbox, coffb, cscore, ccls,
+        x2n, wprep, g_seg0, b_seg0, f0, zerobuf, pbuf);
+
+    nmsmask_comb0_kernel<<<526, 256, 0, stream>>>(coffb, maskb,
+        pbuf, g_seg0, b_seg0, f0);
+
+    nmsserial_resize1_kernel<<<802, 256, 0, stream>>>(cbox, cscore, ccls, maskb,
+        out, roisW, labW, validW, f0, x1n, r1b);
+
     mfma_conv3x3<<<288, 256, 0, stream>>>(r1b, wprep + s0, g_seg1, b_seg1, f1, zerobuf, 512, 256, 40, 40, 0, 4, pbuf);
-    seg_combine_kernel<<<(2*1600*256/4 + 255)/256, 256, 0, stream>>>(pbuf, g_seg1, b_seg1, f1, 4, 2*1600*256/4, 256, 0);
-    resize_add_kernel<<<(2 * 6400 * 32 + 255) / 256, 256, 0, stream>>>(f1, x0n, r2b, 32, 256, 40, 40, 80, 80);
+    seg_combine_kernel<<<800, 256, 0, stream>>>(pbuf, g_seg1, b_seg1, f1, 4, 2*1600*256/4, 256, 0);
+    resize_add_kernel<<<1600, 256, 0, stream>>>(f1, x0n, r2b, 32, 256, 40, 40, 80, 80);
     mfma_conv3x3<<<208, 256, 0, stream>>>(r2b, wprep + s0 + s1, g_seg2, b_seg2, fseg, zerobuf, 256, 128, 80, 80, 0, 2, pbuf);
-    seg_combine_kernel<<<(2*6400*128/4 + 255)/256, 256, 0, stream>>>(pbuf, g_seg2, b_seg2, fseg, 2, 2*6400*128/4, 128, 0);
+    seg_combine_kernel<<<1600, 256, 0, stream>>>(pbuf, g_seg2, b_seg2, fseg, 2, 2*6400*128/4, 128, 0);
 
     for (int d0i = 0; d0i < 200; d0i += DCH) {
         int total = DCH * 784 * 16;
```

Result: slower. 550.9 us (+21.7%).
